# Kernel optimization log

Measured on AMD Instinct MI355X. Metric: run time of the kernel, lower is better.

Reference implementation:

```python
import jax, jax.numpy as jnp
import numpy as np

D = 64
NEG = 0.01            # leakyrelu_neg_slope
X_CONN = 0.25         # x_connection_init
SKIP_H = 0.5          # skip_weight_h
SIGMAS = np.asarray(1.5 ** np.arange(15), np.float32)  # all_sigmas_dist

N_LIG, N_REC = 4096, 8192
E_LIG, E_REC = 65536, 262144
F_LIG, F_REC, NRBF = 15, 27, 15


def _lrelu(x):
    return jax.nn.leaky_relu(x, NEG)


def _ln(x, g, b, eps=1e-5):
    m = x.mean(-1, keepdims=True)
    v = ((x - m) ** 2).mean(-1, keepdims=True)
    return (x - m) * jax.lax.rsqrt(v + eps) * g + b


def _mlp2(x, w1, b1, g, bt, w2, b2):
    # nn.Sequential(Linear, Dropout(0), LeakyReLU, LayerNorm, Linear) in eval mode
    return _ln(_lrelu(x @ w1 + b1), g, bt) @ w2 + b2


def _coords_mlp(m, w1, b1, w2, b2):
    # nn.Sequential(Linear, Dropout(0), LeakyReLU, Linear(out,1))
    return _lrelu(m @ w1 + b1) @ w2 + b2  # [E, 1]


def _seg_mean(v, idx, n):
    # DGL fn.mean over incoming edges at destination nodes (0 for isolated nodes)
    s = jax.ops.segment_sum(v, idx, num_segments=n)
    c = jax.ops.segment_sum(jnp.ones(idx.shape, v.dtype), idx, num_segments=n)
    return s / jnp.maximum(c, 1.0)[:, None]


def setup_inputs() -> dict:
    key = jax.random.key(0)
    ks = iter(jax.random.split(key, 64))

    def n(shape, s=1.0):
        return jax.random.normal(next(ks), shape, jnp.float32) * s

    def lin(i, o):
        return n((i, o), 1.0 / float(np.sqrt(i)))

    zeros = lambda *s: jnp.zeros(s, jnp.float32)
    ones = lambda *s: jnp.ones(s, jnp.float32)

    d = {}
    d['coords_lig'] = n((N_LIG, 3))
    d['h_lig'] = n((N_LIG, D))
    d['orig_h_lig'] = n((N_LIG, D))
    d['orig_coords_lig'] = n((N_LIG, 3))
    d['coords_rec'] = n((N_REC, 3))
    d['h_rec'] = n((N_REC, D))
    d['orig_h_rec'] = n((N_REC, D))
    d['orig_coords_rec'] = n((N_REC, 3))
    d['lig_src'] = jax.random.randint(next(ks), (E_LIG,), 0, N_LIG)
    d['lig_dst'] = jax.random.randint(next(ks), (E_LIG,), 0, N_LIG)
    d['lig_efeat'] = n((E_LIG, F_LIG))
    d['rec_src'] = jax.random.randint(next(ks), (E_REC,), 0, N_REC)
    d['rec_dst'] = jax.random.randint(next(ks), (E_REC,), 0, N_REC)
    d['rec_efeat'] = n((E_REC, F_REC))
    d['mask'] = (jax.random.uniform(next(ks), (N_LIG, N_REC)) < 0.5).astype(jnp.float32)
    # ---- parameters ----
    d['lig_em_w1'], d['lig_em_b1'] = lin(2 * D + F_LIG + NRBF, D), zeros(D)
    d['lig_em_g'], d['lig_em_bt'] = ones(D), zeros(D)
    d['lig_em_w2'], d['lig_em_b2'] = lin(D, D), zeros(D)
    d['rec_em_w1'], d['rec_em_b1'] = lin(2 * D + F_REC + NRBF, D), zeros(D)
    d['rec_em_g'], d['rec_em_bt'] = ones(D), zeros(D)
    d['rec_em_w2'], d['rec_em_b2'] = lin(D, D), zeros(D)
    d['lig_cm_w1'], d['lig_cm_b1'] = lin(D, D), zeros(D)
    d['lig_cm_w2'], d['lig_cm_b2'] = lin(D, 1), zeros(1)
    d['rec_cm_w1'], d['rec_cm_b1'] = lin(D, D), zeros(D)
    d['rec_cm_w2'], d['rec_cm_b2'] = lin(D, 1), zeros(1)
    for nm in ['q_lig_w', 'k_lig_w', 'v_lig_w', 'q_rec_w', 'k_rec_w', 'v_rec_w']:
        d[nm] = lin(D, D)
    d['lig_nm_w1'], d['lig_nm_b1'] = lin(4 * D, D), zeros(D)
    d['lig_nm_g'], d['lig_nm_bt'] = ones(D), zeros(D)
    d['lig_nm_w2'], d['lig_nm_b2'] = lin(D, D), zeros(D)
    d['rec_nm_w1'], d['rec_nm_b1'] = lin(4 * D, D), zeros(D)
    d['rec_nm_g'], d['rec_nm_bt'] = ones(D), zeros(D)
    d['rec_nm_w2'], d['rec_nm_b2'] = lin(D, D), zeros(D)
    return d


def reference(coords_lig, h_lig, orig_h_lig, orig_coords_lig,
              coords_rec, h_rec, orig_h_rec, orig_coords_rec,
              lig_src, lig_dst, lig_efeat, rec_src, rec_dst, rec_efeat, mask,
              lig_em_w1, lig_em_b1, lig_em_g, lig_em_bt, lig_em_w2, lig_em_b2,
              rec_em_w1, rec_em_b1, rec_em_g, rec_em_bt, rec_em_w2, rec_em_b2,
              lig_cm_w1, lig_cm_b1, lig_cm_w2, lig_cm_b2,
              rec_cm_w1, rec_cm_b1, rec_cm_w2, rec_cm_b2,
              q_lig_w, k_lig_w, v_lig_w, q_rec_w, k_rec_w, v_rec_w,
              lig_nm_w1, lig_nm_b1, lig_nm_g, lig_nm_bt, lig_nm_w2, lig_nm_b2,
              rec_nm_w1, rec_nm_b1, rec_nm_g, rec_nm_bt, rec_nm_w2, rec_nm_b2):
    n_lig, n_rec = coords_lig.shape[0], coords_rec.shape[0]
    sig = jnp.asarray(SIGMAS, coords_lig.dtype)

    # --- ligand edge messages: x_rel = x_src - x_dst, multi-scale RBF of |x_rel|^2 ---
    xr_l = coords_lig[lig_src] - coords_lig[lig_dst]                       # [E_l, 3]
    rbf_l = jnp.exp(-jnp.sum(xr_l * xr_l, -1, keepdims=True) / sig)        # [E_l, 15]
    msg_l = _mlp2(jnp.concatenate([h_lig[lig_src], h_lig[lig_dst], lig_efeat, rbf_l], -1),
                  lig_em_w1, lig_em_b1, lig_em_g, lig_em_bt, lig_em_w2, lig_em_b2)

    # --- receptor edge messages (rec_square_distance_scale = 1) ---
    xr_r = coords_rec[rec_src] - coords_rec[rec_dst]
    rbf_r = jnp.exp(-jnp.sum(xr_r * xr_r, -1, keepdims=True) / sig)
    msg_r = _mlp2(jnp.concatenate([h_rec[rec_src], h_rec[rec_dst], rec_efeat, rbf_r], -1),
                  rec_em_w1, rec_em_b1, rec_em_g, rec_em_bt, rec_em_w2, rec_em_b2)

    # --- masked cross-graph attention (pre/post cross-msg norms are identity) ---
    q_l, k_l, v_l = _lrelu(h_lig @ q_lig_w), _lrelu(h_lig @ k_lig_w), h_lig @ v_lig_w
    q_r, k_r, v_r = _lrelu(h_rec @ q_rec_w), _lrelu(h_rec @ k_rec_w), h_rec @ v_rec_w
    s_lr = mask * (q_l @ k_r.T) - 1000.0 * (1.0 - mask)
    att_l = jax.nn.softmax(s_lr, axis=1) @ v_r                             # [N_l, D]
    mt = mask.T
    s_rl = mt * (q_r @ k_l.T) - 1000.0 * (1.0 - mt)
    att_r = jax.nn.softmax(s_rl, axis=1) @ v_l                             # [N_r, D]

    # --- equivariant coordinate update: mean_j phi_x(m_ij) * x_rel, + skip to orig ---
    coef_l = _coords_mlp(msg_l, lig_cm_w1, lig_cm_b1, lig_cm_w2, lig_cm_b2)
    x_lig = X_CONN * orig_coords_lig + (1.0 - X_CONN) * coords_lig + _seg_mean(xr_l * coef_l, lig_dst, n_lig)
    coef_r = _coords_mlp(msg_r, rec_cm_w1, rec_cm_b1, rec_cm_w2, rec_cm_b2)
    x_rec = X_CONN * orig_coords_rec + (1.0 - X_CONN) * coords_rec + _seg_mean(xr_r * coef_r, rec_dst, n_rec)

    # --- node feature update with skip (h_feats_dim == out_feats_dim) ---
    aggr_l = _seg_mean(msg_l, lig_dst, n_lig)
    h_lig_out = SKIP_H * _mlp2(jnp.concatenate([h_lig, aggr_l, att_l, orig_h_lig], -1),
                               lig_nm_w1, lig_nm_b1, lig_nm_g, lig_nm_bt, lig_nm_w2, lig_nm_b2) \
        + (1.0 - SKIP_H) * h_lig
    aggr_r = _seg_mean(msg_r, rec_dst, n_rec)
    h_rec_out = SKIP_H * _mlp2(jnp.concatenate([h_rec, aggr_r, att_r, orig_h_rec], -1),
                               rec_nm_w1, rec_nm_b1, rec_nm_g, rec_nm_bt, rec_nm_w2, rec_nm_b2) \
        + (1.0 - SKIP_H) * h_rec
    return x_lig, h_lig_out, x_rec, h_rec_out
```

## Files before the change

### kernel.cpp

```cpp
#include <hip/hip_runtime.h>
#include <hip/hip_bf16.h>

typedef __hip_bfloat16 bf16;
typedef __attribute__((ext_vector_type(8))) short bfrag8;
typedef __attribute__((ext_vector_type(4))) float f32x4;

#define N_LIG 4096
#define N_REC 8192
#define E_LIG 65536
#define E_REC 262144
#define F_LIGc 15
#define F_RECc 27

__device__ __forceinline__ float ldkv(const float* p, size_t i) { return p[i]; }
__device__ __forceinline__ float ldkv(const bf16* p, size_t i) { return __bfloat162float(p[i]); }
__device__ __forceinline__ short bfbits(float x) {
    bf16 b = __float2bfloat16(x);
    return *(short*)&b;
}
__device__ __forceinline__ unsigned short stg(const float* p, size_t i) {
    return (unsigned short)bfbits(p[i]);
}
__device__ __forceinline__ unsigned short stg(const bf16* p, size_t i) {
    return *(const unsigned short*)(p + i);
}
__device__ __forceinline__ void stage16(unsigned short* d, const bf16* s) {
    *(uint4*)d = *(const uint4*)s;
}
__device__ __forceinline__ void stage16(unsigned short* d, const float* s) {
    float4 a = *(const float4*)s;
    float4 b = *(const float4*)(s + 4);
    unsigned short tmp[8] = {
        (unsigned short)bfbits(a.x), (unsigned short)bfbits(a.y),
        (unsigned short)bfbits(a.z), (unsigned short)bfbits(a.w),
        (unsigned short)bfbits(b.x), (unsigned short)bfbits(b.y),
        (unsigned short)bfbits(b.z), (unsigned short)bfbits(b.w)};
    *(uint4*)d = *(uint4*)tmp;
}

__device__ __forceinline__ int swz(int row, int col) {
    return (row << 6) + ((((col >> 3) ^ row ^ (row >> 3)) & 7) << 3) + (col & 7);
}

__constant__ float c_inv_sigma[15] = {
    1.0f, 0.6666666667f, 0.4444444444f, 0.2962962963f, 0.1975308642f,
    0.1316872428f, 0.08779149520f, 0.05852766346f, 0.03901844231f,
    0.02601229487f, 0.01734152992f, 0.01156101994f, 0.007707346628f,
    0.005138231085f, 0.003425487390f};

__device__ __forceinline__ float wave_sum(float v) {
    #pragma unroll
    for (int o = 32; o > 0; o >>= 1) v += __shfl_xor(v, o, 64);
    return v;
}
__device__ __forceinline__ float quad_max(float v) {
    v = fmaxf(v, __shfl_xor(v, 1)); v = fmaxf(v, __shfl_xor(v, 2));
    v = fmaxf(v, __shfl_xor(v, 4)); v = fmaxf(v, __shfl_xor(v, 8));
    return v;
}
__device__ __forceinline__ float quad_sum(float v) {
    v += __shfl_xor(v, 1); v += __shfl_xor(v, 2);
    v += __shfl_xor(v, 4); v += __shfl_xor(v, 8);
    return v;
}

__global__ void zero_kernel(float* __restrict__ p, int n) {
    int i = blockIdx.x * blockDim.x + threadIdx.x;
    if (i < n) p[i] = 0.f;
}

__global__ void cvt4_kernel(
    const float* __restrict__ a, bf16* __restrict__ oa, int na,
    const float* __restrict__ b, bf16* __restrict__ ob, int nb,
    const float* __restrict__ c, bf16* __restrict__ oc, int nc,
    const float* __restrict__ d, bf16* __restrict__ od, int nd)
{
    int i = blockIdx.x * 256 + threadIdx.x;
    if (i < na) { oa[i] = __float2bfloat16(a[i]); return; }
    i -= na;
    if (i < nb) { ob[i] = __float2bfloat16(b[i]); return; }
    i -= nb;
    if (i < nc) { oc[i] = __float2bfloat16(c[i]); return; }
    i -= nc;
    if (i < nd) od[i] = __float2bfloat16(d[i]);
}

__global__ void hist2_kernel(const int* __restrict__ dl, const int* __restrict__ dr,
                             int* __restrict__ cl, int* __restrict__ cr) {
    int i = blockIdx.x * 256 + threadIdx.x;
    if (i < E_LIG) { atomicAdd(&cl[dl[i]], 1); return; }
    i -= E_LIG;
    if (i < E_REC) atomicAdd(&cr[dr[i]], 1);
}

__global__ __launch_bounds__(256) void scan2_kernel(
    const int* __restrict__ cl, int* __restrict__ curl,
    const int* __restrict__ cr, int* __restrict__ curr)
{
    const int* counts = blockIdx.x ? cr : cl;
    int* cursor = blockIdx.x ? curr : curl;
    int n = blockIdx.x ? N_REC : N_LIG;
    __shared__ int part[256];
    int t = threadIdx.x;
    int c = n / 256;
    int base = t * c;
    int s = 0;
    for (int i = 0; i < c; ++i) s += counts[base + i];
    part[t] = s;
    __syncthreads();
    for (int o = 1; o < 256; o <<= 1) {
        int u = (t >= o) ? part[t - o] : 0;
        __syncthreads();
        part[t] += u;
        __syncthreads();
    }
    int run = part[t] - s;
    for (int i = 0; i < c; ++i) {
        cursor[base + i] = run;
        run += counts[base + i];
    }
}

__global__ void scatter2_kernel(const int* __restrict__ dl, const int* __restrict__ dr,
                                int* __restrict__ curl, int* __restrict__ curr,
                                int* __restrict__ ordl, int* __restrict__ ordr) {
    int i = blockIdx.x * 256 + threadIdx.x;
    if (i < E_LIG) { ordl[atomicAdd(&curl[dl[i]], 1)] = i; return; }
    i -= E_LIG;
    if (i < E_REC) ordr[atomicAdd(&curr[dr[i]], 1)] = i;
}

__global__ __launch_bounds__(256) void pack_frags(
    const float* __restrict__ w_rec1, const float* __restrict__ w_lig1,
    const float* __restrict__ w_rec2, const float* __restrict__ w_lig2,
    const float* __restrict__ c_rec1, const float* __restrict__ c_lig1,
    unsigned short* __restrict__ p_rec1, unsigned short* __restrict__ p_lig1,
    unsigned short* __restrict__ p_rec2, unsigned short* __restrict__ p_lig2,
    unsigned short* __restrict__ pc_rec1, unsigned short* __restrict__ pc_lig1)
{
    int b = blockIdx.x;
    const float* src; unsigned short* dst; int kk, IN;
    if (b < 6)       { src = w_rec1; dst = p_rec1;  kk = b;      IN = 170; }
    else if (b < 11) { src = w_lig1; dst = p_lig1;  kk = b - 6;  IN = 158; }
    else if (b < 13) { src = w_rec2; dst = p_rec2;  kk = b - 11; IN = 64; }
    else if (b < 15) { src = w_lig2; dst = p_lig2;  kk = b - 13; IN = 64; }
    else if (b < 17) { src = c_rec1; dst = pc_rec1; kk = b - 15; IN = 64; }
    else             { src = c_lig1; dst = pc_lig1; kk = b - 17; IN = 64; }
    int t = threadIdx.x, wv = t >> 6, L = t & 63, lm = L & 15, qd = L >> 4;
    int n = wv * 16 + lm;
    unsigned short tmp[8];
    #pragma unroll
    for (int j = 0; j < 8; ++j) {
        int k = kk * 32 + qd * 8 + j;
        tmp[j] = (k < IN) ? (unsigned short)bfbits(src[k * 64 + n]) : (unsigned short)0;
    }
    *(uint4*)&dst[((size_t)(kk * 4 + wv) * 64 + L) * 8] = *(uint4*)tmp;
}

template <int F, int K1S, typename HT>
__global__ __launch_bounds__(256, 5) void edge_mfma(
    const int* __restrict__ order,
    const float* __restrict__ coords, const HT* __restrict__ h,
    const int* __restrict__ src, const int* __restrict__ dst,
    const HT* __restrict__ efeat,
    const unsigned short* __restrict__ w1p, const float* __restrict__ b1,
    const float* __restrict__ g, const float* __restrict__ bt,
    const unsigned short* __restrict__ w2p, const float* __restrict__ b2,
    const unsigned short* __restrict__ c1p, const float* __restrict__ cb1,
    const float* __restrict__ cw2, const float* __restrict__ cb2,
    float* __restrict__ aggr, float* __restrict__ xacc)
{
    constexpr int IN = 143 + F;
    constexpr int KP = K1S * 32 + 8;
    static_assert(64 * KP * 2 >= 64 * 68 * 4, "msgf f32 alias must fit in xb");
    static_assert(64 * KP * 2 >= 64 * 72 * 2, "h1b alias must fit in xb");
    __shared__ __align__(16) char smem[64 * KP * 2];
    __shared__ float wsum1[4][64], wsum2[4][64];
    __shared__ float stat_m[64], stat_r[64];
    __shared__ float coefp[4][64];
    __shared__ float coef_all[64];
    __shared__ int srcs[64], dsts[64], ords[64];
    __shared__ float xr_s[64][3], d2s[64];
    unsigned short* xb   = (unsigned short*)smem;
    unsigned short* h1b  = (unsigned short*)smem;
    float*          msgf = (float*)smem;

    const int t  = threadIdx.x;
    const int wv = t >> 6;
    const int L  = t & 63;
    const int lm = L & 15;
    const int qd = L >> 4;
    const int e0 = blockIdx.x * 64;
    const int n  = wv * 16 + lm;

    bfrag8 w1f[K1S], w2f[2];
    #pragma unroll
    for (int kk = 0; kk < K1S; ++kk)
        w1f[kk] = *(const bfrag8*)&w1p[((size_t)(kk * 4 + wv) * 64 + L) * 8];
    #pragma unroll
    for (int kk = 0; kk < 2; ++kk)
        w2f[kk] = *(const bfrag8*)&w2p[((size_t)(kk * 4 + wv) * 64 + L) * 8];
    const float b1n = b1[n], b2n = b2[n], cb1n = cb1[n], cw2n = cw2[n];
    const float gn = g[n], btn = bt[n];

    if (t < 64) {
        int e = order[e0 + t];
        int s = src[e], d = dst[e];
        ords[t] = e; srcs[t] = s; dsts[t] = d;
        float x0 = coords[s * 3 + 0] - coords[d * 3 + 0];
        float x1 = coords[s * 3 + 1] - coords[d * 3 + 1];
        float x2 = coords[s * 3 + 2] - coords[d * 3 + 2];
        xr_s[t][0] = x0; xr_s[t][1] = x1; xr_s[t][2] = x2;
        d2s[t] = x0 * x0 + x1 * x1 + x2 * x2;
    }
    __syncthreads();

    #pragma unroll
    for (int u = 0; u < 4; ++u) {
        int idx = t + 256 * u;
        int e = idx >> 4, c = idx & 15;
        int node = (c < 8) ? srcs[e] : dsts[e];
        stage16(&xb[e * KP + c * 8], h + (size_t)node * 64 + (c & 7) * 8);
    }
    for (int idx = t; idx < 64 * F; idx += 256) {
        int e = idx / F, f = idx - e * F;
        xb[e * KP + 128 + f] = stg(efeat, (size_t)ords[e] * F + f);
    }
    for (int idx = t; idx < 64 * 15; idx += 256) {
        int e = idx / 15, s5 = idx - e * 15;
        xb[e * KP + 128 + F + s5] = bfbits(__expf(-d2s[e] * c_inv_sigma[s5]));
    }
    {
        constexpr int PER = K1S * 32 - IN;
        for (int idx = t; idx < 64 * PER; idx += 256) {
            int e = idx / PER, k = idx - e * PER;
            xb[e * KP + IN + k] = 0;
        }
    }
    __syncthreads();

    float vreg[4][4];
    #pragma unroll
    for (int m = 0; m < 4; ++m) {
        f32x4 acc = {0.f, 0.f, 0.f, 0.f};
        #pragma unroll
        for (int kk = 0; kk < K1S; ++kk) {
            bfrag8 a = *(const bfrag8*)&xb[(m * 16 + lm) * KP + kk * 32 + qd * 8];
            acc = __builtin_amdgcn_mfma_f32_16x16x32_bf16(a, w1f[kk], acc, 0, 0, 0);
        }
        #pragma unroll
        for (int r = 0; r < 4; ++r) {
            float v = acc[r] + b1n;
            v = v > 0.f ? v : 0.01f * v;
            vreg[m][r] = v;
            float a1 = v, a2 = v * v;
            a1 += __shfl_xor(a1, 1); a2 += __shfl_xor(a2, 1);
            a1 += __shfl_xor(a1, 2); a2 += __shfl_xor(a2, 2);
            a1 += __shfl_xor(a1, 4); a2 += __shfl_xor(a2, 4);
            a1 += __shfl_xor(a1, 8); a2 += __shfl_xor(a2, 8);
            if (lm == 0) {
                wsum1[wv][m * 16 + qd * 4 + r] = a1;
                wsum2[wv][m * 16 + qd * 4 + r] = a2;
            }
        }
    }
    __syncthreads();
    if (t < 64) {
        float s1 = wsum1[0][t] + wsum1[1][t] + wsum1[2][t] + wsum1[3][t];
        float s2 = wsum2[0][t] + wsum2[1][t] + wsum2[2][t] + wsum2[3][t];
        float mean = s1 * (1.f / 64.f);
        float var = s2 * (1.f / 64.f) - mean * mean;
        stat_m[t] = mean;
        stat_r[t] = rsqrtf(fmaxf(var, 0.f) + 1e-5f);
    }
    __syncthreads();

    #pragma unroll
    for (int m = 0; m < 4; ++m)
        #pragma unroll
        for (int r = 0; r < 4; ++r) {
            int row = m * 16 + qd * 4 + r;
            float v = (vreg[m][r] - stat_m[row]) * stat_r[row] * gn + btn;
            h1b[row * 72 + n] = bfbits(v);
        }
    __syncthreads();

    f32x4 acc2[4];
    #pragma unroll
    for (int m = 0; m < 4; ++m) {
        f32x4 acc = {0.f, 0.f, 0.f, 0.f};
        #pragma unroll
        for (int kk = 0; kk < 2; ++kk) {
            bfrag8 a = *(const bfrag8*)&h1b[(m * 16 + lm) * 72 + kk * 32 + qd * 8];
            acc = __builtin_amdgcn_mfma_f32_16x16x32_bf16(a, w2f[kk], acc, 0, 0, 0);
        }
        acc2[m] = acc;
    }
    __syncthreads();
    #pragma unroll
    for (int m = 0; m < 4; ++m)
        #pragma unroll
        for (int r = 0; r < 4; ++r)
            msgf[(m * 16 + qd * 4 + r) * 68 + n] = acc2[m][r] + b2n;
    __syncthreads();

    {
        int j = t & 63, q = t >> 6;
        float acc = 0.f;
        #pragma unroll
        for (int e = q * 16; e < q * 16 + 16; ++e) {
            acc += msgf[e * 68 + j];
            bool flush = (e - q * 16 == 15) || (dsts[e + 1] != dsts[e]);
            if (flush) {
                atomicAdd(&aggr[(size_t)dsts[e] * 64 + j], acc);
                acc = 0.f;
            }
        }
    }

    bfrag8 c1f[2];
    #pragma unroll
    for (int kk = 0; kk < 2; ++kk)
        c1f[kk] = *(const bfrag8*)&c1p[((size_t)(kk * 4 + wv) * 64 + L) * 8];
    #pragma unroll
    for (int m = 0; m < 4; ++m) {
        f32x4 acc = {0.f, 0.f, 0.f, 0.f};
        #pragma unroll
        for (int kk = 0; kk < 2; ++kk) {
            const float* mp = &msgf[(m * 16 + lm) * 68 + kk * 32 + qd * 8];
            f32x4 p0 = *(const f32x4*)mp;
            f32x4 p1 = *(const f32x4*)(mp + 4);
            unsigned short tb[8];
            #pragma unroll
            for (int j = 0; j < 4; ++j) {
                tb[j]     = (unsigned short)bfbits(p0[j]);
                tb[4 + j] = (unsigned short)bfbits(p1[j]);
            }
            bfrag8 a = *(bfrag8*)tb;
            acc = __builtin_amdgcn_mfma_f32_16x16x32_bf16(a, c1f[kk], acc, 0, 0, 0);
        }
        #pragma unroll
        for (int r = 0; r < 4; ++r) {
            float v = acc[r] + cb1n;
            v = v > 0.f ? v : 0.01f * v;
            v *= cw2n;
            v += __shfl_xor(v, 1);
            v += __shfl_xor(v, 2);
            v += __shfl_xor(v, 4);
            v += __shfl_xor(v, 8);
            if (lm == 0) coefp[wv][m * 16 + qd * 4 + r] = v;
        }
    }
    __syncthreads();
    if (t < 64)
        coef_all[t] = coefp[0][t] + coefp[1][t] + coefp[2][t] + coefp[3][t] + cb2[0];
    __syncthreads();

    if (t < 12) {
        int q = t / 3, ax = t - q * 3;
        float acc = 0.f;
        for (int e = q * 16; e < q * 16 + 16; ++e) {
            acc += xr_s[e][ax] * coef_all[e];
            bool flush = (e - q * 16 == 15) || (dsts[e + 1] != dsts[e]);
            if (flush) {
                atomicAdd(&xacc[dsts[e] * 3 + ax], acc);
                acc = 0.f;
            }
        }
    }
}

__global__ __launch_bounds__(256, 3) void node_mfma(
    int nbl,
    const float* h1, const float* __restrict__ aggr1, const int* __restrict__ cnt1,
    const float* att1, const float* __restrict__ origh1,
    const float* __restrict__ w1a, const float* __restrict__ b1a,
    const float* __restrict__ ga, const float* __restrict__ bta,
    const float* __restrict__ w2a, const float* __restrict__ b2a, float* out1,
    const float* h2, const float* __restrict__ aggr2, const int* __restrict__ cnt2,
    const float* att2, const float* __restrict__ origh2,
    const float* __restrict__ w1b, const float* __restrict__ b1b,
    const float* __restrict__ gb, const float* __restrict__ btb,
    const float* __restrict__ w2b, const float* __restrict__ b2b, float* out2)
{
    const float *h, *aggr, *att, *orig_h, *w1, *b1, *g, *bt, *w2, *b2;
    const int* cnt;
    float* h_out;
    int n0;
    if ((int)blockIdx.x < nbl) {
        h = h1; aggr = aggr1; cnt = cnt1; att = att1; orig_h = origh1;
        w1 = w1a; b1 = b1a; g = ga; bt = bta; w2 = w2a; b2 = b2a; h_out = out1;
        n0 = blockIdx.x * 64;
    } else {
        h = h2; aggr = aggr2; cnt = cnt2; att = att2; orig_h = origh2;
        w1 = w1b; b1 = b1b; g = gb; bt = btb; w2 = w2b; b2 = b2b; h_out = out2;
        n0 = (blockIdx.x - nbl) * 64;
    }

    constexpr int KP = 264;
    __shared__ __align__(16) char smem[64 * KP * 2];
    __shared__ __align__(16) unsigned short h1b[64 * 72];
    __shared__ float sums[256], sums2[256];
    __shared__ float stat_m[64], stat_r[64];
    unsigned short* xb  = (unsigned short*)smem;
    float*          h1f = (float*)smem;

    const int t  = threadIdx.x;
    const int lm = t & 15;
    const int qd = (t & 63) >> 4;
    const int n  = (t >> 6) * 16 + lm;

    bfrag8 w1f[8], w2f[2];
    #pragma unroll
    for (int kk = 0; kk < 8; ++kk)
        #pragma unroll
        for (int j = 0; j < 8; ++j) {
            int k = kk * 32 + qd * 8 + j;
            w1f[kk][j] = bfbits(w1[k * 64 + n]);
        }
    #pragma unroll
    for (int kk = 0; kk < 2; ++kk)
        #pragma unroll
        for (int j = 0; j < 8; ++j) {
            int k = kk * 32 + qd * 8 + j;
            w2f[kk][j] = bfbits(w2[k * 64 + n]);
        }
    const float b1n = b1[n], b2n = b2[n];

    for (int p = 0; p < 16; ++p) {
        int e = (t >> 6) + 4 * p;
        int node = n0 + e;
        float invc = 1.f / fmaxf((float)cnt[node], 1.f);
        int j = t & 63;
        xb[e * KP + j]       = bfbits(h[(size_t)node * 64 + j]);
        xb[e * KP + 64 + j]  = bfbits(aggr[(size_t)node * 64 + j] * invc);
        xb[e * KP + 128 + j] = bfbits(att[(size_t)node * 64 + j]);
        xb[e * KP + 192 + j] = bfbits(orig_h[(size_t)node * 64 + j]);
    }
    __syncthreads();

    f32x4 acc1[4];
    #pragma unroll
    for (int m = 0; m < 4; ++m) {
        f32x4 acc = {0.f, 0.f, 0.f, 0.f};
        #pragma unroll
        for (int kk = 0; kk < 8; ++kk) {
            bfrag8 a = *(const bfrag8*)&xb[(m * 16 + lm) * KP + kk * 32 + qd * 8];
            acc = __builtin_amdgcn_mfma_f32_16x16x32_bf16(a, w1f[kk], acc, 0, 0, 0);
        }
        acc1[m] = acc;
    }
    __syncthreads();
    #pragma unroll
    for (int m = 0; m < 4; ++m)
        #pragma unroll
        for (int r = 0; r < 4; ++r) {
            int mr = m * 16 + qd * 4 + r;
            float v = acc1[m][r] + b1n;
            v = v > 0.f ? v : 0.01f * v;
            h1f[mr * 68 + n] = v;
        }
    __syncthreads();

    {
        int e = t >> 2, seg = (t & 3) * 16;
        float s1 = 0.f, s2 = 0.f;
        #pragma unroll
        for (int j = 0; j < 16; ++j) {
            float v = h1f[e * 68 + seg + j];
            s1 += v; s2 += v * v;
        }
        sums[t] = s1; sums2[t] = s2;
    }
    __syncthreads();
    if (t < 64) {
        float s1 = sums[4 * t] + sums[4 * t + 1] + sums[4 * t + 2] + sums[4 * t + 3];
        float s2 = sums2[4 * t] + sums2[4 * t + 1] + sums2[4 * t + 2] + sums2[4 * t + 3];
        float mean = s1 * (1.f / 64.f);
        float var = s2 * (1.f / 64.f) - mean * mean;
        stat_m[t] = mean;
        stat_r[t] = rsqrtf(fmaxf(var, 0.f) + 1e-5f);
    }
    __syncthreads();
    for (int idx = t; idx < 4096; idx += 256) {
        int e = idx >> 6, j = idx & 63;
        float v = (h1f[e * 68 + j] - stat_m[e]) * stat_r[e] * g[j] + bt[j];
        h1b[e * 72 + j] = bfbits(v);
    }
    __syncthreads();

    #pragma unroll
    for (int m = 0; m < 4; ++m) {
        f32x4 acc = {0.f, 0.f, 0.f, 0.f};
        #pragma unroll
        for (int kk = 0; kk < 2; ++kk) {
            bfrag8 a = *(const bfrag8*)&h1b[(m * 16 + lm) * 72 + kk * 32 + qd * 8];
            acc = __builtin_amdgcn_mfma_f32_16x16x32_bf16(a, w2f[kk], acc, 0, 0, 0);
        }
        #pragma unroll
        for (int r = 0; r < 4; ++r) {
            int row = n0 + m * 16 + qd * 4 + r;
            float o = acc[r] + b2n;
            float hv = h[(size_t)row * 64 + n];
            h_out[(size_t)row * 64 + n] = 0.5f * o + 0.5f * hv;
        }
    }
}

__global__ __launch_bounds__(256) void kv_proj_kernel(
    const float* __restrict__ h_lig, const float* __restrict__ h_rec,
    const float* __restrict__ kwl, const float* __restrict__ vwl,
    const float* __restrict__ kwr, const float* __restrict__ vwr,
    bf16* __restrict__ kbl, bf16* __restrict__ vbl,
    bf16* __restrict__ kbr, bf16* __restrict__ vbr)
{
    int job = blockIdx.x * 4 + (threadIdx.x >> 6);
    int j = threadIdx.x & 63;
    const float *h, *w; bf16* out; int node, do_l;
    if (job < N_LIG)                { h = h_lig; w = kwl; out = kbl; node = job;                   do_l = 1; }
    else if (job < 2 * N_LIG)       { h = h_lig; w = vwl; out = vbl; node = job - N_LIG;           do_l = 0; }
    else if (job < 2 * N_LIG + N_REC) { h = h_rec; w = kwr; out = kbr; node = job - 2 * N_LIG;     do_l = 1; }
    else                            { h = h_rec; w = vwr; out = vbr; node = job - 2 * N_LIG - N_REC; do_l = 0; }
    float xv = h[(size_t)node * 64 + j];
    float acc = 0.f;
    #pragma unroll
    for (int i = 0; i < 64; ++i) acc += __shfl(xv, i, 64) * w[i * 64 + j];
    if (do_l) acc = acc > 0.f ? acc : 0.01f * acc;
    out[(size_t)node * 64 + j] = __float2bfloat16(acc);
}

__global__ __launch_bounds__(256) void build_masks(
    const float* __restrict__ mask, unsigned long long* __restrict__ mq,
    unsigned long long* __restrict__ mqT, int R, int C)
{
    __shared__ __align__(4) unsigned char tr[64 * 68];
    __shared__ __align__(4) unsigned char tc[64 * 68];
    int r0 = blockIdx.y * 64, c0 = blockIdx.x * 64;
    int t = threadIdx.x;
    int cs = (t & 15) * 4;
    #pragma unroll
    for (int rr = 0; rr < 4; ++rr) {
        int r = (t >> 4) + rr * 16;
        const float* mp = &mask[(size_t)(r0 + r) * C + c0 + cs];
        unsigned char b0 = mp[0] != 0.f, b1 = mp[1] != 0.f;
        unsigned char b2 = mp[2] != 0.f, b3 = mp[3] != 0.f;
        tr[r * 68 + cs + 0] = b0; tr[r * 68 + cs + 1] = b1;
        tr[r * 68 + cs + 2] = b2; tr[r * 68 + cs + 3] = b3;
        tc[(cs + 0) * 68 + r] = b0; tc[(cs + 1) * 68 + r] = b1;
        tc[(cs + 2) * 68 + r] = b2; tc[(cs + 3) * 68 + r] = b3;
    }
    __syncthreads();
    if (t < 128) {
        const unsigned* p = (t < 64) ? (const unsigned*)&tr[t * 68]
                                     : (const unsigned*)&tc[(t - 64) * 68];
        unsigned lo = 0, hi = 0;
        #pragma unroll
        for (int i = 0; i < 8; ++i)
            lo |= (((p[i] & 0x01010101u) * 0x01020408u) >> 24 & 0xFu) << (4 * i);
        #pragma unroll
        for (int i = 8; i < 16; ++i)
            hi |= (((p[i] & 0x01010101u) * 0x01020408u) >> 24 & 0xFu) << (4 * (i - 8));
        unsigned long long w = (unsigned long long)lo | ((unsigned long long)hi << 32);
        if (t < 64) mq[(size_t)(c0 >> 6) * R + r0 + t] = w;
        else        mqT[(size_t)(r0 >> 6) * C + c0 + (t - 64)] = w;
    }
}

template <int MMODE>
__global__ __launch_bounds__(256, 4) void attn_mfma(
    int nb1,
    const float* __restrict__ h1, const float* __restrict__ qw1,
    const bf16* __restrict__ k1, const bf16* __restrict__ v1,
    const unsigned long long* __restrict__ mq1, const float* __restrict__ mf1, long mrs1, long mcs1,
    float* __restrict__ pO1, float* __restrict__ pM1, float* __restrict__ pL1,
    int nrows1, int ncols1, int nsplit1,
    const float* __restrict__ h2, const float* __restrict__ qw2,
    const bf16* __restrict__ k2, const bf16* __restrict__ v2,
    const unsigned long long* __restrict__ mq2, const float* __restrict__ mf2, long mrs2, long mcs2,
    float* __restrict__ pO2, float* __restrict__ pM2, float* __restrict__ pL2,
    int nrows2, int ncols2, int nsplit2)
{
    const float *h, *qw, *mf;
    const bf16 *kkp, *vvp;
    const unsigned long long* mq;
    long mrs, mcs;
    float *pO, *pM, *pL;
    int n_rows, n_cols, nsplit, bid;
    if ((int)blockIdx.x < nb1) {
        h = h1; qw = qw1; kkp = k1; vvp = v1; mq = mq1; mf = mf1; mrs = mrs1; mcs = mcs1;
        pO = pO1; pM = pM1; pL = pL1; n_rows = nrows1; n_cols = ncols1; nsplit = nsplit1;
        bid = blockIdx.x;
    } else {
        h = h2; qw = qw2; kkp = k2; vvp = v2; mq = mq2; mf = mf2; mrs = mrs2; mcs = mcs2;
        pO = pO2; pM = pM2; pL = pL2; n_rows = nrows2; n_cols = ncols2; nsplit = nsplit2;
        bid = blockIdx.x - nb1;
    }

    const int t  = threadIdx.x;
    const int wv = t >> 6;
    const int lm = t & 15;
    const int qd = (t & 63) >> 4;
    const int rb = bid / nsplit;
    const int sp = bid - rb * nsplit;
    const int r0 = rb * 64;
    const int cols_per = n_cols / nsplit;
    const int c_begin = sp * cols_per;

    __shared__ __align__(16) unsigned short sQ[64 * 64];
    __shared__ __align__(16) unsigned short sP[64 * 64];
    __shared__ __align__(16) unsigned short sK[64 * 64];
    __shared__ __align__(16) unsigned short sV[64 * 64];
    __shared__ uint2 mtq[64];
    __shared__ unsigned char mt[64 * 80];

    const int cP = t >> 3, segP = (t & 7) * 8;

    #pragma unroll
    for (int u = 0; u < 2; ++u) {
        int rr = cP + 32 * u;
        const float* hp = h + (size_t)(r0 + rr) * 64 + segP;
        unsigned short tmp[8];
        #pragma unroll
        for (int j = 0; j < 8; ++j) tmp[j] = bfbits(hp[j]);
        *(uint4*)&sP[swz(rr, segP)] = *(uint4*)tmp;
        const float* qp = qw + (size_t)rr * 64 + segP;
        #pragma unroll
        for (int j = 0; j < 8; ++j) sK[swz(segP + j, rr)] = bfbits(qp[j]);
    }

    uint4 kreg[2], vreg[2];
    unsigned long long mregq = 0;
    kreg[0] = *(const uint4*)(kkp + (size_t)(c_begin + cP) * 64 + segP);
    kreg[1] = *(const uint4*)(kkp + (size_t)(c_begin + cP + 32) * 64 + segP);
    vreg[0] = *(const uint4*)(vvp + (size_t)(c_begin + cP) * 64 + segP);
    vreg[1] = *(const uint4*)(vvp + (size_t)(c_begin + cP + 32) * 64 + segP);
    if (MMODE == 0 && t < 64)
        mregq = mq[(size_t)(c_begin >> 6) * n_rows + r0 + t];
    __syncthreads();

    {
        bfrag8 a0 = *(const bfrag8*)&sP[swz(wv * 16 + lm, qd * 8)];
        bfrag8 a1 = *(const bfrag8*)&sP[swz(wv * 16 + lm, 32 + qd * 8)];
        #pragma unroll
        for (int ns = 0; ns < 4; ++ns) {
            f32x4 acc = {0.f, 0.f, 0.f, 0.f};
            bfrag8 b0 = *(const bfrag8*)&sK[swz(ns * 16 + lm, qd * 8)];
            bfrag8 b1 = *(const bfrag8*)&sK[swz(ns * 16 + lm, 32 + qd * 8)];
            acc = __builtin_amdgcn_mfma_f32_16x16x32_bf16(a0, b0, acc, 0, 0, 0);
            acc = __builtin_amdgcn_mfma_f32_16x16x32_bf16(a1, b1, acc, 0, 0, 0);
            #pragma unroll
            for (int r = 0; r < 4; ++r) {
                float v = acc[r];
                v = v > 0.f ? v : 0.01f * v;
                sQ[swz(wv * 16 + qd * 4 + r, ns * 16 + lm)] = bfbits(v);
            }
        }
    }
    __syncthreads();

    float rm[4], rl[4];
    #pragma unroll
    for (int r = 0; r < 4; ++r) { rm[r] = -1e30f; rl[r] = 0.f; }
    f32x4 o[4];
    #pragma unroll
    for (int ds = 0; ds < 4; ++ds) o[ds] = (f32x4){0.f, 0.f, 0.f, 0.f};

    const int nt = cols_per / 64;
    for (int tile = 0; tile < nt; ++tile) {
        #pragma unroll
        for (int u = 0; u < 2; ++u) {
            int cc = cP + 32 * u;
            *(uint4*)&sK[swz(cc, segP)] = kreg[u];
            unsigned x0 = vreg[u].x, x1 = vreg[u].y, x2 = vreg[u].z, x3 = vreg[u].w;
            sV[swz(segP + 0, cc)] = (unsigned short)x0;
            sV[swz(segP + 1, cc)] = (unsigned short)(x0 >> 16);
            sV[swz(segP + 2, cc)] = (unsigned short)x1;
            sV[swz(segP + 3, cc)] = (unsigned short)(x1 >> 16);
            sV[swz(segP + 4, cc)] = (unsigned short)x2;
            sV[swz(segP + 5, cc)] = (unsigned short)(x2 >> 16);
            sV[swz(segP + 6, cc)] = (unsigned short)x3;
            sV[swz(segP + 7, cc)] = (unsigned short)(x3 >> 16);
        }
        if (MMODE == 0) {
            if (t < 64) mtq[t] = make_uint2((unsigned)mregq, (unsigned)(mregq >> 32));
        } else {
            int c0 = c_begin + tile * 64;
            #pragma unroll
            for (int u = 0; u < 16; ++u) {
                int i = t + 256 * u;
                int r = i >> 6, c = i & 63;
                mt[r * 80 + c] = (unsigned char)(
                    mf[(size_t)(r0 + r) * mrs + (size_t)(c0 + c) * mcs] != 0.f);
            }
        }
        __syncthreads();

        if (tile + 1 < nt) {
            int c0n = c_begin + (tile + 1) * 64;
            kreg[0] = *(const uint4*)(kkp + (size_t)(c0n + cP) * 64 + segP);
            kreg[1] = *(const uint4*)(kkp + (size_t)(c0n + cP + 32) * 64 + segP);
            vreg[0] = *(const uint4*)(vvp + (size_t)(c0n + cP) * 64 + segP);
            vreg[1] = *(const uint4*)(vvp + (size_t)(c0n + cP + 32) * 64 + segP);
            if (MMODE == 0 && t < 64)
                mregq = mq[(size_t)(c0n >> 6) * n_rows + r0 + t];
        }

        f32x4 s[4];
        {
            bfrag8 a0 = *(const bfrag8*)&sQ[swz(wv * 16 + lm, qd * 8)];
            bfrag8 a1 = *(const bfrag8*)&sQ[swz(wv * 16 + lm, 32 + qd * 8)];
            #pragma unroll
            for (int ns = 0; ns < 4; ++ns) {
                f32x4 acc = {0.f, 0.f, 0.f, 0.f};
                bfrag8 b0 = *(const bfrag8*)&sK[swz(ns * 16 + lm, qd * 8)];
                bfrag8 b1 = *(const bfrag8*)&sK[swz(ns * 16 + lm, 32 + qd * 8)];
                acc = __builtin_amdgcn_mfma_f32_16x16x32_bf16(a0, b0, acc, 0, 0, 0);
                acc = __builtin_amdgcn_mfma_f32_16x16x32_bf16(a1, b1, acc, 0, 0, 0);
                s[ns] = acc;
            }
        }

        float alpha[4];
        #pragma unroll
        for (int r = 0; r < 4; ++r) {
            int rloc = wv * 16 + qd * 4 + r;
            float v0, v1, v2, v3;
            if (MMODE == 0) {
                uint2 w = mtq[rloc];
                v0 = (w.x >> lm) & 1        ? s[0][r] : -1000.f;
                v1 = (w.x >> (16 + lm)) & 1 ? s[1][r] : -1000.f;
                v2 = (w.y >> lm) & 1        ? s[2][r] : -1000.f;
                v3 = (w.y >> (16 + lm)) & 1 ? s[3][r] : -1000.f;
            } else {
                v0 = mt[rloc * 80 +  0 + lm] ? s[0][r] : -1000.f;
                v1 = mt[rloc * 80 + 16 + lm] ? s[1][r] : -1000.f;
                v2 = mt[rloc * 80 + 32 + lm] ? s[2][r] : -1000.f;
                v3 = mt[rloc * 80 + 48 + lm] ? s[3][r] : -1000.f;
            }
            float mx = quad_max(fmaxf(fmaxf(v0, v1), fmaxf(v2, v3)));
            float mn = fmaxf(rm[r], mx);
            float al = __expf(rm[r] - mn);
            rm[r] = mn; alpha[r] = al;
            float p0 = __expf(v0 - mn), p1 = __expf(v1 - mn);
            float p2 = __expf(v2 - mn), p3 = __expf(v3 - mn);
            sP[swz(rloc,  0 + lm)] = bfbits(p0);
            sP[swz(rloc, 16 + lm)] = bfbits(p1);
            sP[swz(rloc, 32 + lm)] = bfbits(p2);
            sP[swz(rloc, 48 + lm)] = bfbits(p3);
            float ls = quad_sum(p0 + p1 + p2 + p3);
            rl[r] = rl[r] * al + ls;
        }
        #pragma unroll
        for (int ds = 0; ds < 4; ++ds)
            #pragma unroll
            for (int r = 0; r < 4; ++r) o[ds][r] *= alpha[r];

        __builtin_amdgcn_wave_barrier();
        asm volatile("" ::: "memory");

        {
            bfrag8 a0 = *(const bfrag8*)&sP[swz(wv * 16 + lm, qd * 8)];
            bfrag8 a1 = *(const bfrag8*)&sP[swz(wv * 16 + lm, 32 + qd * 8)];
            #pragma unroll
            for (int ds = 0; ds < 4; ++ds) {
                bfrag8 b0 = *(const bfrag8*)&sV[swz(ds * 16 + lm, qd * 8)];
                bfrag8 b1 = *(const bfrag8*)&sV[swz(ds * 16 + lm, 32 + qd * 8)];
                o[ds] = __builtin_amdgcn_mfma_f32_16x16x32_bf16(a0, b0, o[ds], 0, 0, 0);
                o[ds] = __builtin_amdgcn_mfma_f32_16x16x32_bf16(a1, b1, o[ds], 0, 0, 0);
            }
        }
        __syncthreads();
    }

    #pragma unroll
    for (int ds = 0; ds < 4; ++ds)
        #pragma unroll
        for (int r = 0; r < 4; ++r) {
            int row = r0 + wv * 16 + qd * 4 + r;
            pO[((size_t)sp * n_rows + row) * 64 + ds * 16 + lm] = o[ds][r];
        }
    if (lm == 0) {
        #pragma unroll
        for (int r = 0; r < 4; ++r) {
            int row = r0 + wv * 16 + qd * 4 + r;
            pM[(size_t)sp * n_rows + row] = rm[r];
            pL[(size_t)sp * n_rows + row] = rl[r];
        }
    }
}

__global__ __launch_bounds__(64) void attn_merge2(
    const float* __restrict__ pO1, const float* __restrict__ pM1, const float* __restrict__ pL1,
    float* __restrict__ out1, int ns1,
    const float* __restrict__ pO2, const float* __restrict__ pM2, const float* __restrict__ pL2,
    float* __restrict__ out2, int ns2)
{
    int r = blockIdx.x;
    const float *pO, *pM, *pL; float* out; int n_rows, nsplit;
    if (r < N_LIG) { pO = pO1; pM = pM1; pL = pL1; out = out1; n_rows = N_LIG; nsplit = ns1; }
    else { r -= N_LIG; pO = pO2; pM = pM2; pL = pL2; out = out2; n_rows = N_REC; nsplit = ns2; }
    int d = threadIdx.x;
    float mstar = -1e30f;
    for (int s = 0; s < nsplit; ++s) mstar = fmaxf(mstar, pM[(size_t)s * n_rows + r]);
    float L = 0.f, O = 0.f;
    for (int s = 0; s < nsplit; ++s) {
        float w = __expf(pM[(size_t)s * n_rows + r] - mstar);
        L += pL[(size_t)s * n_rows + r] * w;
        O += pO[((size_t)s * n_rows + r) * 64 + d] * w;
    }
    out[(size_t)r * 64 + d] = O / L;
}

__global__ __launch_bounds__(256) void attn_row_kernel(
    const float* __restrict__ h, const float* __restrict__ qw,
    const bf16* __restrict__ k, const bf16* __restrict__ v,
    const float* __restrict__ mask, long mrs, long mcs,
    float* __restrict__ out, int n_cols)
{
    int row = blockIdx.x;
    int tid = threadIdx.x;
    extern __shared__ float sc[];
    __shared__ float hrow[64];
    __shared__ float qrow[64];
    __shared__ float red[4];
    __shared__ float opart[4][64];

    if (tid < 64) hrow[tid] = h[(size_t)row * 64 + tid];
    __syncthreads();
    if (tid < 64) {
        float a = 0.f;
        #pragma unroll 8
        for (int i = 0; i < 64; ++i) a += hrow[i] * qw[i * 64 + tid];
        qrow[tid] = a > 0.f ? a : 0.01f * a;
    }
    __syncthreads();

    float lmax = -1e30f;
    for (int c = tid; c < n_cols; c += 256) {
        const bf16* kr = k + (size_t)c * 64;
        float s = 0.f;
        #pragma unroll 8
        for (int i = 0; i < 64; ++i) s += qrow[i] * ldkv(kr, i);
        float m = mask[(size_t)row * mrs + (size_t)c * mcs];
        s = m * s - 1000.f * (1.f - m);
        sc[c] = s;
        lmax = fmaxf(lmax, s);
    }
    #pragma unroll
    for (int o = 32; o > 0; o >>= 1) lmax = fmaxf(lmax, __shfl_xor(lmax, o, 64));
    int wid = tid >> 6;
    if ((tid & 63) == 0) red[wid] = lmax;
    __syncthreads();
    float bmax = fmaxf(fmaxf(red[0], red[1]), fmaxf(red[2], red[3]));
    __syncthreads();

    float lsum = 0.f;
    for (int c = tid; c < n_cols; c += 256) {
        float e = __expf(sc[c] - bmax);
        sc[c] = e;
        lsum += e;
    }
    lsum = wave_sum(lsum);
    if ((tid & 63) == 0) red[wid] = lsum;
    __syncthreads();
    float inv = 1.f / (red[0] + red[1] + red[2] + red[3]);

    int dd = tid & 63;
    float o = 0.f;
    for (int c = wid; c < n_cols; c += 4) o += sc[c] * ldkv(v, (size_t)c * 64 + dd);
    opart[wid][dd] = o;
    __syncthreads();
    if (wid == 0)
        out[(size_t)row * 64 + dd] =
            (opart[0][dd] + opart[1][dd] + opart[2][dd] + opart[3][dd]) * inv;
}

__global__ void coord2_kernel(
    const float* __restrict__ ol, const float* __restrict__ cl,
    const float* __restrict__ xl, const int* __restrict__ cntl, float* __restrict__ outl,
    const float* __restrict__ orr, const float* __restrict__ cr,
    const float* __restrict__ xr, const int* __restrict__ cntr, float* __restrict__ outr)
{
    int i = blockIdx.x * 256 + threadIdx.x;
    if (i < N_LIG * 3) {
        int node = i / 3;
        float invc = 1.f / fmaxf((float)cntl[node], 1.f);
        outl[i] = 0.25f * ol[i] + 0.75f * cl[i] + xl[i] * invc;
        return;
    }
    i -= N_LIG * 3;
    if (i < N_REC * 3) {
        int node = i / 3;
        float invc = 1.f / fmaxf((float)cntr[node], 1.f);
        outr[i] = 0.25f * orr[i] + 0.75f * cr[i] + xr[i] * invc;
    }
}

extern "C" void kernel_launch(void* const* d_in, const int* in_sizes, int n_in,
                              void* d_out, int out_size, void* d_ws, size_t ws_size,
                              hipStream_t stream)
{
    const float* coords_lig      = (const float*)d_in[0];
    const float* h_lig           = (const float*)d_in[1];
    const float* orig_h_lig      = (const float*)d_in[2];
    const float* orig_coords_lig = (const float*)d_in[3];
    const float* coords_rec      = (const float*)d_in[4];
    const float* h_rec           = (const float*)d_in[5];
    const float* orig_h_rec      = (const float*)d_in[6];
    const float* orig_coords_rec = (const float*)d_in[7];
    const int* lig_src   = (const int*)d_in[8];
    const int* lig_dst   = (const int*)d_in[9];
    const float* lig_efeat = (const float*)d_in[10];
    const int* rec_src   = (const int*)d_in[11];
    const int* rec_dst   = (const int*)d_in[12];
    const float* rec_efeat = (const float*)d_in[13];
    const float* mask      = (const float*)d_in[14];
    const float *lig_em_w1 = (const float*)d_in[15], *lig_em_b1 = (const float*)d_in[16];
    const float *lig_em_g  = (const float*)d_in[17], *lig_em_bt = (const float*)d_in[18];
    const float *lig_em_w2 = (const float*)d_in[19], *lig_em_b2 = (const float*)d_in[20];
    const float *rec_em_w1 = (const float*)d_in[21], *rec_em_b1 = (const float*)d_in[22];
    const float *rec_em_g  = (const float*)d_in[23], *rec_em_bt = (const float*)d_in[24];
    const float *rec_em_w2 = (const float*)d_in[25], *rec_em_b2 = (const float*)d_in[26];
    const float *lig_cm_w1 = (const float*)d_in[27], *lig_cm_b1 = (const float*)d_in[28];
    const float *lig_cm_w2 = (const float*)d_in[29], *lig_cm_b2 = (const float*)d_in[30];
    const float *rec_cm_w1 = (const float*)d_in[31], *rec_cm_b1 = (const float*)d_in[32];
    const float *rec_cm_w2 = (const float*)d_in[33], *rec_cm_b2 = (const float*)d_in[34];
    const float *q_lig_w = (const float*)d_in[35], *k_lig_w = (const float*)d_in[36];
    const float *v_lig_w = (const float*)d_in[37], *q_rec_w = (const float*)d_in[38];
    const float *k_rec_w = (const float*)d_in[39], *v_rec_w = (const float*)d_in[40];
    const float *lig_nm_w1 = (const float*)d_in[41], *lig_nm_b1 = (const float*)d_in[42];
    const float *lig_nm_g  = (const float*)d_in[43], *lig_nm_bt = (const float*)d_in[44];
    const float *lig_nm_w2 = (const float*)d_in[45], *lig_nm_b2 = (const float*)d_in[46];
    const float *rec_nm_w1 = (const float*)d_in[47], *rec_nm_b1 = (const float*)d_in[48];
    const float *rec_nm_g  = (const float*)d_in[49], *rec_nm_bt = (const float*)d_in[50];
    const float *rec_nm_w2 = (const float*)d_in[51], *rec_nm_b2 = (const float*)d_in[52];

    char* wsb = (char*)d_ws;
    float* aggr_l = (float*)(wsb + 16);
    float* aggr_r = aggr_l + (size_t)N_LIG * 64;
    float* xacc_l = aggr_r + (size_t)N_REC * 64;
    float* xacc_r = xacc_l + (size_t)N_LIG * 3;
    int* counts_l = (int*)(xacc_r + (size_t)N_REC * 3);
    int* counts_r = counts_l + N_LIG;
    const size_t zero_floats =
        (size_t)N_LIG * 64 + (size_t)N_REC * 64 + N_LIG * 3 + N_REC * 3 + N_LIG + N_REC;
    int* cursor_l = counts_r + N_REC;
    int* cursor_r = cursor_l + N_LIG;
    int* order_l  = cursor_r + N_REC;
    int* order_r  = order_l + E_LIG;
    unsigned short* p_rec1  = (unsigned short*)(order_r + E_REC);
    unsigned short* p_lig1  = p_rec1 + 6 * 2048;
    unsigned short* p_rec2  = p_lig1 + 5 * 2048;
    unsigned short* p_lig2  = p_rec2 + 2 * 2048;
    unsigned short* pc_rec1 = p_lig2 + 2 * 2048;
    unsigned short* pc_lig1 = pc_rec1 + 2 * 2048;
    char* kv_base = (char*)(pc_lig1 + 2 * 2048);
    const size_t core_b = (size_t)(kv_base - wsb);
    const size_t kv_b = (size_t)(N_LIG + N_REC) * 64 * 2 * 2;

    const size_t mq1_n = (size_t)(N_REC / 64) * N_LIG;
    const size_t mq2_n = (size_t)(N_LIG / 64) * N_REC;
    const size_t mq_all_b = (mq1_n + mq2_n) * 8;
    const size_t mir_b = (size_t)(N_LIG + N_REC) * 64 * 2
                       + ((size_t)E_LIG * F_LIGc + (size_t)E_REC * F_RECc) * 2;
    const size_t region_b = mir_b > mq_all_b ? mir_b : mq_all_b;

    const size_t part_b_hi = ((size_t)8 * N_LIG * 64 + (size_t)4 * N_REC * 64) * 4
                           + ((size_t)8 * N_LIG + (size_t)4 * N_REC) * 2 * 4;
    const size_t part_b_lo = ((size_t)4 * N_LIG * 64 + (size_t)2 * N_REC * 64) * 4
                           + ((size_t)4 * N_LIG + (size_t)2 * N_REC) * 2 * 4;

    int tier, ns1, ns2;
    size_t part_b;
    if (ws_size >= core_b + kv_b + part_b_hi + region_b) {
        tier = 0; ns1 = 8; ns2 = 4; part_b = part_b_hi;
    } else if (ws_size >= core_b + kv_b + part_b_lo + region_b) {
        tier = 0; ns1 = 4; ns2 = 2; part_b = part_b_lo;
    } else if (ws_size >= core_b + kv_b + part_b_lo) {
        tier = 1; ns1 = 4; ns2 = 2; part_b = part_b_lo;
    } else {
        tier = 2; ns1 = 4; ns2 = 2; part_b = part_b_lo;
    }

    bf16* kb_l = (bf16*)kv_base;
    bf16* vb_l = kb_l + (size_t)N_LIG * 64;
    bf16* kb_r = vb_l + (size_t)N_LIG * 64;
    bf16* vb_r = kb_r + (size_t)N_REC * 64;
    float* pO1 = (float*)(kv_base + kv_b);
    float* pO2 = pO1 + (size_t)ns1 * N_LIG * 64;
    float* pM1 = pO2 + (size_t)ns2 * N_REC * 64;
    float* pL1 = pM1 + (size_t)ns1 * N_LIG;
    float* pM2 = pL1 + (size_t)ns1 * N_LIG;
    float* pL2 = pM2 + (size_t)ns2 * N_REC;
    unsigned long long* mqb  = (unsigned long long*)(kv_base + kv_b + part_b);
    unsigned long long* mqbT = mqb + mq1_n;
    bf16* hb_l  = (bf16*)mqb;
    bf16* hb_r  = hb_l + (size_t)N_LIG * 64;
    bf16* efb_l = hb_r + (size_t)N_REC * 64;
    bf16* efb_r = efb_l + (size_t)E_LIG * F_LIGc;

    float* out = (float*)d_out;
    float* x_lig_o = out;
    float* h_lig_o = out + 12288;
    float* x_rec_o = out + 274432;
    float* h_rec_o = out + 299008;

    zero_kernel<<<((int)zero_floats + 255) / 256, 256, 0, stream>>>(aggr_l, (int)zero_floats);

    pack_frags<<<19, 256, 0, stream>>>(
        rec_em_w1, lig_em_w1, rec_em_w2, lig_em_w2, rec_cm_w1, lig_cm_w1,
        p_rec1, p_lig1, p_rec2, p_lig2, pc_rec1, pc_lig1);

    hist2_kernel<<<(E_LIG + E_REC) / 256, 256, 0, stream>>>(lig_dst, rec_dst, counts_l, counts_r);
    scan2_kernel<<<2, 256, 0, stream>>>(counts_l, cursor_l, counts_r, cursor_r);
    scatter2_kernel<<<(E_LIG + E_REC) / 256, 256, 0, stream>>>(
        lig_dst, rec_dst, cursor_l, cursor_r, order_l, order_r);

    kv_proj_kernel<<<(2 * (N_LIG + N_REC)) / 4, 256, 0, stream>>>(
        h_lig, h_rec, k_lig_w, v_lig_w, k_rec_w, v_rec_w,
        kb_l, vb_l, kb_r, vb_r);

    if (tier == 0) {
        cvt4_kernel<<<(N_LIG * 64 + N_REC * 64 + E_LIG * F_LIGc + E_REC * F_RECc + 255) / 256,
                      256, 0, stream>>>(
            h_lig, hb_l, N_LIG * 64, h_rec, hb_r, N_REC * 64,
            lig_efeat, efb_l, E_LIG * F_LIGc, rec_efeat, efb_r, E_REC * F_RECc);
        edge_mfma<F_LIGc, 5, bf16><<<E_LIG / 64, 256, 0, stream>>>(
            order_l, coords_lig, hb_l, lig_src, lig_dst, efb_l,
            p_lig1, lig_em_b1, lig_em_g, lig_em_bt, p_lig2, lig_em_b2,
            pc_lig1, lig_cm_b1, lig_cm_w2, lig_cm_b2,
            aggr_l, xacc_l);
        edge_mfma<F_RECc, 6, bf16><<<E_REC / 64, 256, 0, stream>>>(
            order_r, coords_rec, hb_r, rec_src, rec_dst, efb_r,
            p_rec1, rec_em_b1, rec_em_g, rec_em_bt, p_rec2, rec_em_b2,
            pc_rec1, rec_cm_b1, rec_cm_w2, rec_cm_b2,
            aggr_r, xacc_r);
    } else {
        edge_mfma<F_LIGc, 5, float><<<E_LIG / 64, 256, 0, stream>>>(
            order_l, coords_lig, h_lig, lig_src, lig_dst, lig_efeat,
            p_lig1, lig_em_b1, lig_em_g, lig_em_bt, p_lig2, lig_em_b2,
            pc_lig1, lig_cm_b1, lig_cm_w2, lig_cm_b2,
            aggr_l, xacc_l);
        edge_mfma<F_RECc, 6, float><<<E_REC / 64, 256, 0, stream>>>(
            order_r, coords_rec, h_rec, rec_src, rec_dst, rec_efeat,
            p_rec1, rec_em_b1, rec_em_g, rec_em_bt, p_rec2, rec_em_b2,
            pc_rec1, rec_cm_b1, rec_cm_w2, rec_cm_b2,
            aggr_r, xacc_r);
    }

    const int nb1 = (N_LIG / 64) * ns1;
    const int nb2 = (N_REC / 64) * ns2;
    if (tier <= 1) {
        if (tier == 0) {
            dim3 bg(N_REC / 64, N_LIG / 64);
            build_masks<<<bg, 256, 0, stream>>>(mask, mqb, mqbT, N_LIG, N_REC);
            attn_mfma<0><<<nb1 + nb2, 256, 0, stream>>>(
                nb1,
                h_lig, q_lig_w, kb_r, vb_r, mqb, mask, 0L, 0L,
                pO1, pM1, pL1, N_LIG, N_REC, ns1,
                h_rec, q_rec_w, kb_l, vb_l, mqbT, mask, 0L, 0L,
                pO2, pM2, pL2, N_REC, N_LIG, ns2);
        } else {
            attn_mfma<1><<<nb1 + nb2, 256, 0, stream>>>(
                nb1,
                h_lig, q_lig_w, kb_r, vb_r, (const unsigned long long*)0, mask, (long)N_REC, 1L,
                pO1, pM1, pL1, N_LIG, N_REC, ns1,
                h_rec, q_rec_w, kb_l, vb_l, (const unsigned long long*)0, mask, 1L, (long)N_REC,
                pO2, pM2, pL2, N_REC, N_LIG, ns2);
        }
        attn_merge2<<<N_LIG + N_REC, 64, 0, stream>>>(
            pO1, pM1, pL1, h_lig_o, ns1, pO2, pM2, pL2, h_rec_o, ns2);
    } else {
        attn_row_kernel<<<N_LIG, 256, N_REC * sizeof(float), stream>>>(
            h_lig, q_lig_w, kb_r, vb_r, mask, (long)N_REC, 1L, h_lig_o, N_REC);
        attn_row_kernel<<<N_REC, 256, N_LIG * sizeof(float), stream>>>(
            h_rec, q_rec_w, kb_l, vb_l, mask, 1L, (long)N_REC, h_rec_o, N_LIG);
    }

    node_mfma<<<N_LIG / 64 + N_REC / 64, 256, 0, stream>>>(
        N_LIG / 64,
        h_lig, aggr_l, counts_l, h_lig_o, orig_h_lig,
        lig_nm_w1, lig_nm_b1, lig_nm_g, lig_nm_bt, lig_nm_w2, lig_nm_b2, h_lig_o,
        h_rec, aggr_r, counts_r, h_rec_o, orig_h_rec,
        rec_nm_w1, rec_nm_b1, rec_nm_g, rec_nm_bt, rec_nm_w2, rec_nm_b2, h_rec_o);

    coord2_kernel<<<((N_LIG + N_REC) * 3 + 255) / 256, 256, 0, stream>>>(
        orig_coords_lig, coords_lig, xacc_l, counts_l, x_lig_o,
        orig_coords_rec, coords_rec, xacc_r, counts_r, x_rec_o);
}
```

Measured before the change: 608.4 us.

## Fuse edge and attention work into one persistent mega kernel with shared smem

Turns the edge MLP and masked attention kernels into device functions that share one dynamic shared buffer, and launches them from a single mega_kernel so the edge and attention blocks run concurrently on the GPU. The attention row-sum is now computed with an extra MFMA against a ones vector instead of shuffle reductions. The split count for attention doubles, build_masks moves earlier, and the coordinate update is folded into node_mfma. The aim is to remove launch gaps and tail underutilisation. The cost is higher register and LDS pressure from the merged kernel, plus extra partial buffers to merge.

```diff
diff --git a/kernel.cpp b/kernel.cpp
--- a/kernel.cpp
+++ b/kernel.cpp
@@ -56,11 +56,6 @@
 __device__ __forceinline__ float quad_max(float v) {
     v = fmaxf(v, __shfl_xor(v, 1)); v = fmaxf(v, __shfl_xor(v, 2));
     v = fmaxf(v, __shfl_xor(v, 4)); v = fmaxf(v, __shfl_xor(v, 8));
-    return v;
-}
-__device__ __forceinline__ float quad_sum(float v) {
-    v += __shfl_xor(v, 1); v += __shfl_xor(v, 2);
-    v += __shfl_xor(v, 4); v += __shfl_xor(v, 8);
     return v;
 }
 
@@ -158,7 +153,8 @@
 }
 
 template <int F, int K1S, typename HT>
-__global__ __launch_bounds__(256, 5) void edge_mfma(
+__device__ __forceinline__ void edge_body(
+    char* sbuf, int ebid,
     const int* __restrict__ order,
     const float* __restrict__ coords, const HT* __restrict__ h,
     const int* __restrict__ src, const int* __restrict__ dst,
@@ -172,25 +168,30 @@
 {
     constexpr int IN = 143 + F;
     constexpr int KP = K1S * 32 + 8;
-    static_assert(64 * KP * 2 >= 64 * 68 * 4, "msgf f32 alias must fit in xb");
-    static_assert(64 * KP * 2 >= 64 * 72 * 2, "h1b alias must fit in xb");
-    __shared__ __align__(16) char smem[64 * KP * 2];
-    __shared__ float wsum1[4][64], wsum2[4][64];
-    __shared__ float stat_m[64], stat_r[64];
-    __shared__ float coefp[4][64];
-    __shared__ float coef_all[64];
-    __shared__ int srcs[64], dsts[64], ords[64];
-    __shared__ float xr_s[64][3], d2s[64];
-    unsigned short* xb   = (unsigned short*)smem;
-    unsigned short* h1b  = (unsigned short*)smem;
-    float*          msgf = (float*)smem;
+    constexpr int XB = 64 * KP * 2;
+    static_assert(XB >= 64 * 68 * 4, "msgf f32 alias must fit in xb");
+    static_assert(XB >= 64 * 72 * 2, "h1b alias must fit in xb");
+    unsigned short* xb   = (unsigned short*)sbuf;
+    unsigned short* h1b  = (unsigned short*)sbuf;
+    float*          msgf = (float*)sbuf;
+    float* wsum1   = (float*)(sbuf + XB);
+    float* wsum2   = (float*)(sbuf + XB + 1024);
+    float* stat_m  = (float*)(sbuf + XB + 2048);
+    float* stat_r  = (float*)(sbuf + XB + 2304);
+    float* coefp   = (float*)(sbuf + XB + 2560);
+    float* coef_all= (float*)(sbuf + XB + 3584);
+    int*   srcs    = (int*)(sbuf + XB + 3840);
+    int*   dsts    = (int*)(sbuf + XB + 4096);
+    int*   ords    = (int*)(sbuf + XB + 4352);
+    float* xr_s    = (float*)(sbuf + XB + 4608);
+    float* d2s     = (float*)(sbuf + XB + 5376);
 
     const int t  = threadIdx.x;
     const int wv = t >> 6;
     const int L  = t & 63;
     const int lm = L & 15;
     const int qd = L >> 4;
-    const int e0 = blockIdx.x * 64;
+    const int e0 = ebid * 64;
     const int n  = wv * 16 + lm;
 
     bfrag8 w1f[K1S], w2f[2];
@@ -210,7 +211,7 @@
         float x0 = coords[s * 3 + 0] - coords[d * 3 + 0];
         float x1 = coords[s * 3 + 1] - coords[d * 3 + 1];
         float x2 = coords[s * 3 + 2] - coords[d * 3 + 2];
-        xr_s[t][0] = x0; xr_s[t][1] = x1; xr_s[t][2] = x2;
+        xr_s[t * 3 + 0] = x0; xr_s[t * 3 + 1] = x1; xr_s[t * 3 + 2] = x2;
         d2s[t] = x0 * x0 + x1 * x1 + x2 * x2;
     }
     __syncthreads();
@@ -259,15 +260,15 @@
             a1 += __shfl_xor(a1, 4); a2 += __shfl_xor(a2, 4);
             a1 += __shfl_xor(a1, 8); a2 += __shfl_xor(a2, 8);
             if (lm == 0) {
-                wsum1[wv][m * 16 + qd * 4 + r] = a1;
-                wsum2[wv][m * 16 + qd * 4 + r] = a2;
+                wsum1[wv * 64 + m * 16 + qd * 4 + r] = a1;
+                wsum2[wv * 64 + m * 16 + qd * 4 + r] = a2;
             }
         }
     }
     __syncthreads();
     if (t < 64) {
-        float s1 = wsum1[0][t] + wsum1[1][t] + wsum1[2][t] + wsum1[3][t];
-        float s2 = wsum2[0][t] + wsum2[1][t] + wsum2[2][t] + wsum2[3][t];
+        float s1 = wsum1[t] + wsum1[64 + t] + wsum1[128 + t] + wsum1[192 + t];
+        float s2 = wsum2[t] + wsum2[64 + t] + wsum2[128 + t] + wsum2[192 + t];
         float mean = s1 * (1.f / 64.f);
         float var = s2 * (1.f / 64.f) - mean * mean;
         stat_m[t] = mean;
@@ -348,19 +349,19 @@
             v += __shfl_xor(v, 2);
             v += __shfl_xor(v, 4);
             v += __shfl_xor(v, 8);
-            if (lm == 0) coefp[wv][m * 16 + qd * 4 + r] = v;
+            if (lm == 0) coefp[wv * 64 + m * 16 + qd * 4 + r] = v;
         }
     }
     __syncthreads();
     if (t < 64)
-        coef_all[t] = coefp[0][t] + coefp[1][t] + coefp[2][t] + coefp[3][t] + cb2[0];
+        coef_all[t] = coefp[t] + coefp[64 + t] + coefp[128 + t] + coefp[192 + t] + cb2[0];
     __syncthreads();
 
     if (t < 12) {
         int q = t / 3, ax = t - q * 3;
         float acc = 0.f;
         for (int e = q * 16; e < q * 16 + 16; ++e) {
-            acc += xr_s[e][ax] * coef_all[e];
+            acc += xr_s[e * 3 + ax] * coef_all[e];
             bool flush = (e - q * 16 == 15) || (dsts[e + 1] != dsts[e]);
             if (flush) {
                 atomicAdd(&xacc[dsts[e] * 3 + ax], acc);
@@ -370,205 +371,9 @@
     }
 }
 
-__global__ __launch_bounds__(256, 3) void node_mfma(
-    int nbl,
-    const float* h1, const float* __restrict__ aggr1, const int* __restrict__ cnt1,
-    const float* att1, const float* __restrict__ origh1,
-    const float* __restrict__ w1a, const float* __restrict__ b1a,
-    const float* __restrict__ ga, const float* __restrict__ bta,
-    const float* __restrict__ w2a, const float* __restrict__ b2a, float* out1,
-    const float* h2, const float* __restrict__ aggr2, const int* __restrict__ cnt2,
-    const float* att2, const float* __restrict__ origh2,
-    const float* __restrict__ w1b, const float* __restrict__ b1b,
-    const float* __restrict__ gb, const float* __restrict__ btb,
-    const float* __restrict__ w2b, const float* __restrict__ b2b, float* out2)
-{
-    const float *h, *aggr, *att, *orig_h, *w1, *b1, *g, *bt, *w2, *b2;
-    const int* cnt;
-    float* h_out;
-    int n0;
-    if ((int)blockIdx.x < nbl) {
-        h = h1; aggr = aggr1; cnt = cnt1; att = att1; orig_h = origh1;
-        w1 = w1a; b1 = b1a; g = ga; bt = bta; w2 = w2a; b2 = b2a; h_out = out1;
-        n0 = blockIdx.x * 64;
-    } else {
-        h = h2; aggr = aggr2; cnt = cnt2; att = att2; orig_h = origh2;
-        w1 = w1b; b1 = b1b; g = gb; bt = btb; w2 = w2b; b2 = b2b; h_out = out2;
-        n0 = (blockIdx.x - nbl) * 64;
-    }
-
-    constexpr int KP = 264;
-    __shared__ __align__(16) char smem[64 * KP * 2];
-    __shared__ __align__(16) unsigned short h1b[64 * 72];
-    __shared__ float sums[256], sums2[256];
-    __shared__ float stat_m[64], stat_r[64];
-    unsigned short* xb  = (unsigned short*)smem;
-    float*          h1f = (float*)smem;
-
-    const int t  = threadIdx.x;
-    const int lm = t & 15;
-    const int qd = (t & 63) >> 4;
-    const int n  = (t >> 6) * 16 + lm;
-
-    bfrag8 w1f[8], w2f[2];
-    #pragma unroll
-    for (int kk = 0; kk < 8; ++kk)
-        #pragma unroll
-        for (int j = 0; j < 8; ++j) {
-            int k = kk * 32 + qd * 8 + j;
-            w1f[kk][j] = bfbits(w1[k * 64 + n]);
-        }
-    #pragma unroll
-    for (int kk = 0; kk < 2; ++kk)
-        #pragma unroll
-        for (int j = 0; j < 8; ++j) {
-            int k = kk * 32 + qd * 8 + j;
-            w2f[kk][j] = bfbits(w2[k * 64 + n]);
-        }
-    const float b1n = b1[n], b2n = b2[n];
-
-    for (int p = 0; p < 16; ++p) {
-        int e = (t >> 6) + 4 * p;
-        int node = n0 + e;
-        float invc = 1.f / fmaxf((float)cnt[node], 1.f);
-        int j = t & 63;
-        xb[e * KP + j]       = bfbits(h[(size_t)node * 64 + j]);
-        xb[e * KP + 64 + j]  = bfbits(aggr[(size_t)node * 64 + j] * invc);
-        xb[e * KP + 128 + j] = bfbits(att[(size_t)node * 64 + j]);
-        xb[e * KP + 192 + j] = bfbits(orig_h[(size_t)node * 64 + j]);
-    }
-    __syncthreads();
-
-    f32x4 acc1[4];
-    #pragma unroll
-    for (int m = 0; m < 4; ++m) {
-        f32x4 acc = {0.f, 0.f, 0.f, 0.f};
-        #pragma unroll
-        for (int kk = 0; kk < 8; ++kk) {
-            bfrag8 a = *(const bfrag8*)&xb[(m * 16 + lm) * KP + kk * 32 + qd * 8];
-            acc = __builtin_amdgcn_mfma_f32_16x16x32_bf16(a, w1f[kk], acc, 0, 0, 0);
-        }
-        acc1[m] = acc;
-    }
-    __syncthreads();
-    #pragma unroll
-    for (int m = 0; m < 4; ++m)
-        #pragma unroll
-        for (int r = 0; r < 4; ++r) {
-            int mr = m * 16 + qd * 4 + r;
-            float v = acc1[m][r] + b1n;
-            v = v > 0.f ? v : 0.01f * v;
-            h1f[mr * 68 + n] = v;
-        }
-    __syncthreads();
-
-    {
-        int e = t >> 2, seg = (t & 3) * 16;
-        float s1 = 0.f, s2 = 0.f;
-        #pragma unroll
-        for (int j = 0; j < 16; ++j) {
-            float v = h1f[e * 68 + seg + j];
-            s1 += v; s2 += v * v;
-        }
-        sums[t] = s1; sums2[t] = s2;
-    }
-    __syncthreads();
-    if (t < 64) {
-        float s1 = sums[4 * t] + sums[4 * t + 1] + sums[4 * t + 2] + sums[4 * t + 3];
-        float s2 = sums2[4 * t] + sums2[4 * t + 1] + sums2[4 * t + 2] + sums2[4 * t + 3];
-        float mean = s1 * (1.f / 64.f);
-        float var = s2 * (1.f / 64.f) - mean * mean;
-        stat_m[t] = mean;
-        stat_r[t] = rsqrtf(fmaxf(var, 0.f) + 1e-5f);
-    }
-    __syncthreads();
-    for (int idx = t; idx < 4096; idx += 256) {
-        int e = idx >> 6, j = idx & 63;
-        float v = (h1f[e * 68 + j] - stat_m[e]) * stat_r[e] * g[j] + bt[j];
-        h1b[e * 72 + j] = bfbits(v);
-    }
-    __syncthreads();
-
-    #pragma unroll
-    for (int m = 0; m < 4; ++m) {
-        f32x4 acc = {0.f, 0.f, 0.f, 0.f};
-        #pragma unroll
-        for (int kk = 0; kk < 2; ++kk) {
-            bfrag8 a = *(const bfrag8*)&h1b[(m * 16 + lm) * 72 + kk * 32 + qd * 8];
-            acc = __builtin_amdgcn_mfma_f32_16x16x32_bf16(a, w2f[kk], acc, 0, 0, 0);
-        }
-        #pragma unroll
-        for (int r = 0; r < 4; ++r) {
-            int row = n0 + m * 16 + qd * 4 + r;
-            float o = acc[r] + b2n;
-            float hv = h[(size_t)row * 64 + n];
-            h_out[(size_t)row * 64 + n] = 0.5f * o + 0.5f * hv;
-        }
-    }
-}
-
-__global__ __launch_bounds__(256) void kv_proj_kernel(
-    const float* __restrict__ h_lig, const float* __restrict__ h_rec,
-    const float* __restrict__ kwl, const float* __restrict__ vwl,
-    const float* __restrict__ kwr, const float* __restrict__ vwr,
-    bf16* __restrict__ kbl, bf16* __restrict__ vbl,
-    bf16* __restrict__ kbr, bf16* __restrict__ vbr)
-{
-    int job = blockIdx.x * 4 + (threadIdx.x >> 6);
-    int j = threadIdx.x & 63;
-    const float *h, *w; bf16* out; int node, do_l;
-    if (job < N_LIG)                { h = h_lig; w = kwl; out = kbl; node = job;                   do_l = 1; }
-    else if (job < 2 * N_LIG)       { h = h_lig; w = vwl; out = vbl; node = job - N_LIG;           do_l = 0; }
-    else if (job < 2 * N_LIG + N_REC) { h = h_rec; w = kwr; out = kbr; node = job - 2 * N_LIG;     do_l = 1; }
-    else                            { h = h_rec; w = vwr; out = vbr; node = job - 2 * N_LIG - N_REC; do_l = 0; }
-    float xv = h[(size_t)node * 64 + j];
-    float acc = 0.f;
-    #pragma unroll
-    for (int i = 0; i < 64; ++i) acc += __shfl(xv, i, 64) * w[i * 64 + j];
-    if (do_l) acc = acc > 0.f ? acc : 0.01f * acc;
-    out[(size_t)node * 64 + j] = __float2bfloat16(acc);
-}
-
-__global__ __launch_bounds__(256) void build_masks(
-    const float* __restrict__ mask, unsigned long long* __restrict__ mq,
-    unsigned long long* __restrict__ mqT, int R, int C)
-{
-    __shared__ __align__(4) unsigned char tr[64 * 68];
-    __shared__ __align__(4) unsigned char tc[64 * 68];
-    int r0 = blockIdx.y * 64, c0 = blockIdx.x * 64;
-    int t = threadIdx.x;
-    int cs = (t & 15) * 4;
-    #pragma unroll
-    for (int rr = 0; rr < 4; ++rr) {
-        int r = (t >> 4) + rr * 16;
-        const float* mp = &mask[(size_t)(r0 + r) * C + c0 + cs];
-        unsigned char b0 = mp[0] != 0.f, b1 = mp[1] != 0.f;
-        unsigned char b2 = mp[2] != 0.f, b3 = mp[3] != 0.f;
-        tr[r * 68 + cs + 0] = b0; tr[r * 68 + cs + 1] = b1;
-        tr[r * 68 + cs + 2] = b2; tr[r * 68 + cs + 3] = b3;
-        tc[(cs + 0) * 68 + r] = b0; tc[(cs + 1) * 68 + r] = b1;
-        tc[(cs + 2) * 68 + r] = b2; tc[(cs + 3) * 68 + r] = b3;
-    }
-    __syncthreads();
-    if (t < 128) {
-        const unsigned* p = (t < 64) ? (const unsigned*)&tr[t * 68]
-                                     : (const unsigned*)&tc[(t - 64) * 68];
-        unsigned lo = 0, hi = 0;
-        #pragma unroll
-        for (int i = 0; i < 8; ++i)
-            lo |= (((p[i] & 0x01010101u) * 0x01020408u) >> 24 & 0xFu) << (4 * i);
-        #pragma unroll
-        for (int i = 8; i < 16; ++i)
-            hi |= (((p[i] & 0x01010101u) * 0x01020408u) >> 24 & 0xFu) << (4 * (i - 8));
-        unsigned long long w = (unsigned long long)lo | ((unsigned long long)hi << 32);
-        if (t < 64) mq[(size_t)(c0 >> 6) * R + r0 + t] = w;
-        else        mqT[(size_t)(r0 >> 6) * C + c0 + (t - 64)] = w;
-    }
-}
-
 template <int MMODE>
-__global__ __launch_bounds__(256, 4) void attn_mfma(
-    int nb1,
+__device__ __forceinline__ void attn_body(
+    char* sbuf, int bid, int nb1,
     const float* __restrict__ h1, const float* __restrict__ qw1,
     const bf16* __restrict__ k1, const bf16* __restrict__ v1,
     const unsigned long long* __restrict__ mq1, const float* __restrict__ mf1, long mrs1, long mcs1,
@@ -585,16 +390,22 @@
     const unsigned long long* mq;
     long mrs, mcs;
     float *pO, *pM, *pL;
-    int n_rows, n_cols, nsplit, bid;
-    if ((int)blockIdx.x < nb1) {
+    int n_rows, n_cols, nsplit;
+    if (bid < nb1) {
         h = h1; qw = qw1; kkp = k1; vvp = v1; mq = mq1; mf = mf1; mrs = mrs1; mcs = mcs1;
         pO = pO1; pM = pM1; pL = pL1; n_rows = nrows1; n_cols = ncols1; nsplit = nsplit1;
-        bid = blockIdx.x;
     } else {
         h = h2; qw = qw2; kkp = k2; vvp = v2; mq = mq2; mf = mf2; mrs = mrs2; mcs = mcs2;
         pO = pO2; pM = pM2; pL = pL2; n_rows = nrows2; n_cols = ncols2; nsplit = nsplit2;
-        bid = blockIdx.x - nb1;
-    }
+        bid -= nb1;
+    }
+
+    unsigned short* sQ = (unsigned short*)sbuf;
+    unsigned short* sP = (unsigned short*)(sbuf + 8192);
+    unsigned short* sK = (unsigned short*)(sbuf + 16384);
+    unsigned short* sV = (unsigned short*)(sbuf + 24576);
+    uint2* mtq = (uint2*)(sbuf + 32768);
+    unsigned char* mt = (unsigned char*)(sbuf + 32768);
 
     const int t  = threadIdx.x;
     const int wv = t >> 6;
@@ -605,13 +416,6 @@
     const int r0 = rb * 64;
     const int cols_per = n_cols / nsplit;
     const int c_begin = sp * cols_per;
-
-    __shared__ __align__(16) unsigned short sQ[64 * 64];
-    __shared__ __align__(16) unsigned short sP[64 * 64];
-    __shared__ __align__(16) unsigned short sK[64 * 64];
-    __shared__ __align__(16) unsigned short sV[64 * 64];
-    __shared__ uint2 mtq[64];
-    __shared__ unsigned char mt[64 * 80];
 
     const int cP = t >> 3, segP = (t & 7) * 8;
 
@@ -658,12 +462,15 @@
     }
     __syncthreads();
 
-    float rm[4], rl[4];
-    #pragma unroll
-    for (int r = 0; r < 4; ++r) { rm[r] = -1e30f; rl[r] = 0.f; }
+    float rm[4];
+    #pragma unroll
+    for (int r = 0; r < 4; ++r) rm[r] = -1e30f;
     f32x4 o[4];
     #pragma unroll
     for (int ds = 0; ds < 4; ++ds) o[ds] = (f32x4){0.f, 0.f, 0.f, 0.f};
+    f32x4 osum = {0.f, 0.f, 0.f, 0.f};
+    const short ONE = (short)0x3F80;
+    const bfrag8 bones = {ONE, ONE, ONE, ONE, ONE, ONE, ONE, ONE};
 
     const int nt = cols_per / 64;
     for (int tile = 0; tile < nt; ++tile) {
@@ -747,8 +554,7 @@
             sP[swz(rloc, 16 + lm)] = bfbits(p1);
             sP[swz(rloc, 32 + lm)] = bfbits(p2);
             sP[swz(rloc, 48 + lm)] = bfbits(p3);
-            float ls = quad_sum(p0 + p1 + p2 + p3);
-            rl[r] = rl[r] * al + ls;
+            osum[r] *= al;
         }
         #pragma unroll
         for (int ds = 0; ds < 4; ++ds)
@@ -768,6 +574,8 @@
                 o[ds] = __builtin_amdgcn_mfma_f32_16x16x32_bf16(a0, b0, o[ds], 0, 0, 0);
                 o[ds] = __builtin_amdgcn_mfma_f32_16x16x32_bf16(a1, b1, o[ds], 0, 0, 0);
             }
+            osum = __builtin_amdgcn_mfma_f32_16x16x32_bf16(a0, bones, osum, 0, 0, 0);
+            osum = __builtin_amdgcn_mfma_f32_16x16x32_bf16(a1, bones, osum, 0, 0, 0);
         }
         __syncthreads();
     }
@@ -784,8 +592,295 @@
         for (int r = 0; r < 4; ++r) {
             int row = r0 + wv * 16 + qd * 4 + r;
             pM[(size_t)sp * n_rows + row] = rm[r];
-            pL[(size_t)sp * n_rows + row] = rl[r];
-        }
+            pL[(size_t)sp * n_rows + row] = osum[r];
+        }
+    }
+}
+
+__global__ __launch_bounds__(256, 4) void mega_kernel(
+    int nb1,
+    const float* h1, const float* qw1, const bf16* k1, const bf16* v1,
+    const unsigned long long* mq1, float* pO1, float* pM1, float* pL1,
+    int nrows1, int ncols1, int ns1,
+    const float* h2, const float* qw2, const bf16* k2, const bf16* v2,
+    const unsigned long long* mq2, float* pO2, float* pM2, float* pL2,
+    int nrows2, int ncols2, int ns2,
+    const int* ordR, const float* coordsR, const bf16* hR,
+    const int* srcR, const int* dstR, const bf16* efR,
+    const unsigned short* w1pR, const float* b1R, const float* gR, const float* btR,
+    const unsigned short* w2pR, const float* b2R,
+    const unsigned short* c1pR, const float* cb1R, const float* cw2R, const float* cb2R,
+    float* aggrR, float* xaccR,
+    const int* ordL, const float* coordsL, const bf16* hL,
+    const int* srcL, const int* dstL, const bf16* efL,
+    const unsigned short* w1pL, const float* b1L, const float* gL, const float* btL,
+    const unsigned short* w2pL, const float* b2L,
+    const unsigned short* c1pL, const float* cb1L, const float* cw2L, const float* cb2L,
+    float* aggrL, float* xaccL)
+{
+    __shared__ __align__(16) char sbuf[33280];
+    int bid = blockIdx.x;
+    int g7 = bid / 7, r7 = bid - g7 * 7;
+    if (r7 < 2) {
+        attn_body<0>(sbuf, g7 * 2 + r7, nb1,
+            h1, qw1, k1, v1, mq1, (const float*)0, 0L, 0L, pO1, pM1, pL1, nrows1, ncols1, ns1,
+            h2, qw2, k2, v2, mq2, (const float*)0, 0L, 0L, pO2, pM2, pL2, nrows2, ncols2, ns2);
+    } else {
+        int eid = g7 * 5 + (r7 - 2);
+        if (eid < E_REC / 64)
+            edge_body<F_RECc, 6, bf16>(sbuf, eid, ordR, coordsR, hR, srcR, dstR, efR,
+                w1pR, b1R, gR, btR, w2pR, b2R, c1pR, cb1R, cw2R, cb2R, aggrR, xaccR);
+        else
+            edge_body<F_LIGc, 5, bf16>(sbuf, eid - E_REC / 64, ordL, coordsL, hL, srcL, dstL, efL,
+                w1pL, b1L, gL, btL, w2pL, b2L, c1pL, cb1L, cw2L, cb2L, aggrL, xaccL);
+    }
+}
+
+template <int F, int K1S>
+__global__ __launch_bounds__(256, 4) void edge_mfma_f(
+    const int* order, const float* coords, const float* h,
+    const int* src, const int* dst, const float* efeat,
+    const unsigned short* w1p, const float* b1, const float* g, const float* bt,
+    const unsigned short* w2p, const float* b2,
+    const unsigned short* c1p, const float* cb1, const float* cw2, const float* cb2,
+    float* aggr, float* xacc)
+{
+    __shared__ __align__(16) char sbuf[64 * (K1S * 32 + 8) * 2 + 5632];
+    edge_body<F, K1S, float>(sbuf, blockIdx.x, order, coords, h, src, dst, efeat,
+        w1p, b1, g, bt, w2p, b2, c1p, cb1, cw2, cb2, aggr, xacc);
+}
+
+__global__ __launch_bounds__(256, 4) void attn_f32mask(
+    int nb1,
+    const float* h1, const float* qw1, const bf16* k1, const bf16* v1,
+    const float* mf1, long mrs1, long mcs1,
+    float* pO1, float* pM1, float* pL1, int nrows1, int ncols1, int ns1,
+    const float* h2, const float* qw2, const bf16* k2, const bf16* v2,
+    const float* mf2, long mrs2, long mcs2,
+    float* pO2, float* pM2, float* pL2, int nrows2, int ncols2, int ns2)
+{
+    __shared__ __align__(16) char sbuf[37888];
+    attn_body<1>(sbuf, blockIdx.x, nb1,
+        h1, qw1, k1, v1, (const unsigned long long*)0, mf1, mrs1, mcs1,
+        pO1, pM1, pL1, nrows1, ncols1, ns1,
+        h2, qw2, k2, v2, (const unsigned long long*)0, mf2, mrs2, mcs2,
+        pO2, pM2, pL2, nrows2, ncols2, ns2);
+}
+
+__global__ __launch_bounds__(256, 3) void node_mfma(
+    int nbl, int nbn,
+    const float* h1, const float* __restrict__ aggr1, const int* __restrict__ cnt1,
+    const float* att1, const float* __restrict__ origh1,
+    const float* __restrict__ w1a, const float* __restrict__ b1a,
+    const float* __restrict__ ga, const float* __restrict__ bta,
+    const float* __restrict__ w2a, const float* __restrict__ b2a, float* out1,
+    const float* h2, const float* __restrict__ aggr2, const int* __restrict__ cnt2,
+    const float* att2, const float* __restrict__ origh2,
+    const float* __restrict__ w1b, const float* __restrict__ b1b,
+    const float* __restrict__ gb, const float* __restrict__ btb,
+    const float* __restrict__ w2b, const float* __restrict__ b2b, float* out2,
+    const float* __restrict__ ocl, const float* __restrict__ ccl,
+    const float* __restrict__ xaccl, float* __restrict__ outxl,
+    const float* __restrict__ ocr, const float* __restrict__ ccr,
+    const float* __restrict__ xaccr, float* __restrict__ outxr)
+{
+    if ((int)blockIdx.x >= nbn) {
+        int i = (blockIdx.x - nbn) * 256 + threadIdx.x;
+        if (i < N_LIG * 3) {
+            int node = i / 3;
+            float invc = 1.f / fmaxf((float)cnt1[node], 1.f);
+            outxl[i] = 0.25f * ocl[i] + 0.75f * ccl[i] + xaccl[i] * invc;
+        } else {
+            i -= N_LIG * 3;
+            if (i < N_REC * 3) {
+                int node = i / 3;
+                float invc = 1.f / fmaxf((float)cnt2[node], 1.f);
+                outxr[i] = 0.25f * ocr[i] + 0.75f * ccr[i] + xaccr[i] * invc;
+            }
+        }
+        return;
+    }
+
+    const float *h, *aggr, *att, *orig_h, *w1, *b1, *g, *bt, *w2, *b2;
+    const int* cnt;
+    float* h_out;
+    int n0;
+    if ((int)blockIdx.x < nbl) {
+        h = h1; aggr = aggr1; cnt = cnt1; att = att1; orig_h = origh1;
+        w1 = w1a; b1 = b1a; g = ga; bt = bta; w2 = w2a; b2 = b2a; h_out = out1;
+        n0 = blockIdx.x * 64;
+    } else {
+        h = h2; aggr = aggr2; cnt = cnt2; att = att2; orig_h = origh2;
+        w1 = w1b; b1 = b1b; g = gb; bt = btb; w2 = w2b; b2 = b2b; h_out = out2;
+        n0 = (blockIdx.x - nbl) * 64;
+    }
+
+    constexpr int KP = 264;
+    __shared__ __align__(16) char smem[64 * KP * 2];
+    __shared__ __align__(16) unsigned short h1b[64 * 72];
+    __shared__ float sums[256], sums2[256];
+    __shared__ float stat_m[64], stat_r[64];
+    unsigned short* xb  = (unsigned short*)smem;
+    float*          h1f = (float*)smem;
+
+    const int t  = threadIdx.x;
+    const int lm = t & 15;
+    const int qd = (t & 63) >> 4;
+    const int n  = (t >> 6) * 16 + lm;
+
+    bfrag8 w1f[8], w2f[2];
+    #pragma unroll
+    for (int kk = 0; kk < 8; ++kk)
+        #pragma unroll
+        for (int j = 0; j < 8; ++j) {
+            int k = kk * 32 + qd * 8 + j;
+            w1f[kk][j] = bfbits(w1[k * 64 + n]);
+        }
+    #pragma unroll
+    for (int kk = 0; kk < 2; ++kk)
+        #pragma unroll
+        for (int j = 0; j < 8; ++j) {
+            int k = kk * 32 + qd * 8 + j;
+            w2f[kk][j] = bfbits(w2[k * 64 + n]);
+        }
+    const float b1n = b1[n], b2n = b2[n];
+
+    for (int p = 0; p < 16; ++p) {
+        int e = (t >> 6) + 4 * p;
+        int node = n0 + e;
+        float invc = 1.f / fmaxf((float)cnt[node], 1.f);
+        int j = t & 63;
+        xb[e * KP + j]       = bfbits(h[(size_t)node * 64 + j]);
+        xb[e * KP + 64 + j]  = bfbits(aggr[(size_t)node * 64 + j] * invc);
+        xb[e * KP + 128 + j] = bfbits(att[(size_t)node * 64 + j]);
+        xb[e * KP + 192 + j] = bfbits(orig_h[(size_t)node * 64 + j]);
+    }
+    __syncthreads();
+
+    f32x4 acc1[4];
+    #pragma unroll
+    for (int m = 0; m < 4; ++m) {
+        f32x4 acc = {0.f, 0.f, 0.f, 0.f};
+        #pragma unroll
+        for (int kk = 0; kk < 8; ++kk) {
+            bfrag8 a = *(const bfrag8*)&xb[(m * 16 + lm) * KP + kk * 32 + qd * 8];
+            acc = __builtin_amdgcn_mfma_f32_16x16x32_bf16(a, w1f[kk], acc, 0, 0, 0);
+        }
+        acc1[m] = acc;
+    }
+    __syncthreads();
+    #pragma unroll
+    for (int m = 0; m < 4; ++m)
+        #pragma unroll
+        for (int r = 0; r < 4; ++r) {
+            int mr = m * 16 + qd * 4 + r;
+            float v = acc1[m][r] + b1n;
+            v = v > 0.f ? v : 0.01f * v;
+            h1f[mr * 68 + n] = v;
+        }
+    __syncthreads();
+
+    {
+        int e = t >> 2, seg = (t & 3) * 16;
+        float s1 = 0.f, s2 = 0.f;
+        #pragma unroll
+        for (int j = 0; j < 16; ++j) {
+            float v = h1f[e * 68 + seg + j];
+            s1 += v; s2 += v * v;
+        }
+        sums[t] = s1; sums2[t] = s2;
+    }
+    __syncthreads();
+    if (t < 64) {
+        float s1 = sums[4 * t] + sums[4 * t + 1] + sums[4 * t + 2] + sums[4 * t + 3];
+        float s2 = sums2[4 * t] + sums2[4 * t + 1] + sums2[4 * t + 2] + sums2[4 * t + 3];
+        float mean = s1 * (1.f / 64.f);
+        float var = s2 * (1.f / 64.f) - mean * mean;
+        stat_m[t] = mean;
+        stat_r[t] = rsqrtf(fmaxf(var, 0.f) + 1e-5f);
+    }
+    __syncthreads();
+    for (int idx = t; idx < 4096; idx += 256) {
+        int e = idx >> 6, j = idx & 63;
+        float v = (h1f[e * 68 + j] - stat_m[e]) * stat_r[e] * g[j] + bt[j];
+        h1b[e * 72 + j] = bfbits(v);
+    }
+    __syncthreads();
+
+    #pragma unroll
+    for (int m = 0; m < 4; ++m) {
+        f32x4 acc = {0.f, 0.f, 0.f, 0.f};
+        #pragma unroll
+        for (int kk = 0; kk < 2; ++kk) {
+            bfrag8 a = *(const bfrag8*)&h1b[(m * 16 + lm) * 72 + kk * 32 + qd * 8];
+            acc = __builtin_amdgcn_mfma_f32_16x16x32_bf16(a, w2f[kk], acc, 0, 0, 0);
+        }
+        #pragma unroll
+        for (int r = 0; r < 4; ++r) {
+            int row = n0 + m * 16 + qd * 4 + r;
+            float o = acc[r] + b2n;
+            float hv = h[(size_t)row * 64 + n];
+            h_out[(size_t)row * 64 + n] = 0.5f * o + 0.5f * hv;
+        }
+    }
+}
+
+__global__ __launch_bounds__(256) void kv_proj_kernel(
+    const float* __restrict__ h_lig, const float* __restrict__ h_rec,
+    const float* __restrict__ kwl, const float* __restrict__ vwl,
+    const float* __restrict__ kwr, const float* __restrict__ vwr,
+    bf16* __restrict__ kbl, bf16* __restrict__ vbl,
+    bf16* __restrict__ kbr, bf16* __restrict__ vbr)
+{
+    int job = blockIdx.x * 4 + (threadIdx.x >> 6);
+    int j = threadIdx.x & 63;
+    const float *h, *w; bf16* out; int node, do_l;
+    if (job < N_LIG)                { h = h_lig; w = kwl; out = kbl; node = job;                   do_l = 1; }
+    else if (job < 2 * N_LIG)       { h = h_lig; w = vwl; out = vbl; node = job - N_LIG;           do_l = 0; }
+    else if (job < 2 * N_LIG + N_REC) { h = h_rec; w = kwr; out = kbr; node = job - 2 * N_LIG;     do_l = 1; }
+    else                            { h = h_rec; w = vwr; out = vbr; node = job - 2 * N_LIG - N_REC; do_l = 0; }
+    float xv = h[(size_t)node * 64 + j];
+    float acc = 0.f;
+    #pragma unroll
+    for (int i = 0; i < 64; ++i) acc += __shfl(xv, i, 64) * w[i * 64 + j];
+    if (do_l) acc = acc > 0.f ? acc : 0.01f * acc;
+    out[(size_t)node * 64 + j] = __float2bfloat16(acc);
+}
+
+__global__ __launch_bounds__(256) void build_masks(
+    const float* __restrict__ mask, unsigned long long* __restrict__ mq,
+    unsigned long long* __restrict__ mqT, int R, int C)
+{
+    __shared__ __align__(4) unsigned char tr[64 * 68];
+    __shared__ __align__(4) unsigned char tc[64 * 68];
+    int r0 = blockIdx.y * 64, c0 = blockIdx.x * 64;
+    int t = threadIdx.x;
+    int cs = (t & 15) * 4;
+    #pragma unroll
+    for (int rr = 0; rr < 4; ++rr) {
+        int r = (t >> 4) + rr * 16;
+        const float* mp = &mask[(size_t)(r0 + r) * C + c0 + cs];
+        unsigned char b0 = mp[0] != 0.f, b1 = mp[1] != 0.f;
+        unsigned char b2 = mp[2] != 0.f, b3 = mp[3] != 0.f;
+        tr[r * 68 + cs + 0] = b0; tr[r * 68 + cs + 1] = b1;
+        tr[r * 68 + cs + 2] = b2; tr[r * 68 + cs + 3] = b3;
+        tc[(cs + 0) * 68 + r] = b0; tc[(cs + 1) * 68 + r] = b1;
+        tc[(cs + 2) * 68 + r] = b2; tc[(cs + 3) * 68 + r] = b3;
+    }
+    __syncthreads();
+    if (t < 128) {
+        const unsigned* p = (t < 64) ? (const unsigned*)&tr[t * 68]
+                                     : (const unsigned*)&tc[(t - 64) * 68];
+        unsigned lo = 0, hi = 0;
+        #pragma unroll
+        for (int i = 0; i < 8; ++i)
+            lo |= (((p[i] & 0x01010101u) * 0x01020408u) >> 24 & 0xFu) << (4 * i);
+        #pragma unroll
+        for (int i = 8; i < 16; ++i)
+            hi |= (((p[i] & 0x01010101u) * 0x01020408u) >> 24 & 0xFu) << (4 * (i - 8));
+        unsigned long long w = (unsigned long long)lo | ((unsigned long long)hi << 32);
+        if (t < 64) mq[(size_t)(c0 >> 6) * R + r0 + t] = w;
+        else        mqT[(size_t)(r0 >> 6) * C + c0 + (t - 64)] = w;
     }
 }
 
@@ -873,27 +968,6 @@
     if (wid == 0)
         out[(size_t)row * 64 + dd] =
             (opart[0][dd] + opart[1][dd] + opart[2][dd] + opart[3][dd]) * inv;
-}
-
-__global__ void coord2_kernel(
-    const float* __restrict__ ol, const float* __restrict__ cl,
-    const float* __restrict__ xl, const int* __restrict__ cntl, float* __restrict__ outl,
-    const float* __restrict__ orr, const float* __restrict__ cr,
-    const float* __restrict__ xr, const int* __restrict__ cntr, float* __restrict__ outr)
-{
-    int i = blockIdx.x * 256 + threadIdx.x;
-    if (i < N_LIG * 3) {
-        int node = i / 3;
-        float invc = 1.f / fmaxf((float)cntl[node], 1.f);
-        outl[i] = 0.25f * ol[i] + 0.75f * cl[i] + xl[i] * invc;
-        return;
-    }
-    i -= N_LIG * 3;
-    if (i < N_REC * 3) {
-        int node = i / 3;
-        float invc = 1.f / fmaxf((float)cntr[node], 1.f);
-        outr[i] = 0.25f * orr[i] + 0.75f * cr[i] + xr[i] * invc;
-    }
 }
 
 extern "C" void kernel_launch(void* const* d_in, const int* in_sizes, int n_in,
@@ -963,19 +1037,16 @@
     const size_t mq_all_b = (mq1_n + mq2_n) * 8;
     const size_t mir_b = (size_t)(N_LIG + N_REC) * 64 * 2
                        + ((size_t)E_LIG * F_LIGc + (size_t)E_REC * F_RECc) * 2;
-    const size_t region_b = mir_b > mq_all_b ? mir_b : mq_all_b;
-
-    const size_t part_b_hi = ((size_t)8 * N_LIG * 64 + (size_t)4 * N_REC * 64) * 4
-                           + ((size_t)8 * N_LIG + (size_t)4 * N_REC) * 2 * 4;
+
+    const size_t part_b_hi = ((size_t)16 * N_LIG * 64 + (size_t)8 * N_REC * 64) * 4
+                           + ((size_t)16 * N_LIG + (size_t)8 * N_REC) * 2 * 4;
     const size_t part_b_lo = ((size_t)4 * N_LIG * 64 + (size_t)2 * N_REC * 64) * 4
                            + ((size_t)4 * N_LIG + (size_t)2 * N_REC) * 2 * 4;
 
     int tier, ns1, ns2;
     size_t part_b;
-    if (ws_size >= core_b + kv_b + part_b_hi + region_b) {
-        tier = 0; ns1 = 8; ns2 = 4; part_b = part_b_hi;
-    } else if (ws_size >= core_b + kv_b + part_b_lo + region_b) {
-        tier = 0; ns1 = 4; ns2 = 2; part_b = part_b_lo;
+    if (ws_size >= core_b + kv_b + part_b_hi + mq_all_b + mir_b) {
+        tier = 0; ns1 = 16; ns2 = 8; part_b = part_b_hi;
     } else if (ws_size >= core_b + kv_b + part_b_lo) {
         tier = 1; ns1 = 4; ns2 = 2; part_b = part_b_lo;
     } else {
@@ -994,7 +1065,7 @@
     float* pL2 = pM2 + (size_t)ns2 * N_REC;
     unsigned long long* mqb  = (unsigned long long*)(kv_base + kv_b + part_b);
     unsigned long long* mqbT = mqb + mq1_n;
-    bf16* hb_l  = (bf16*)mqb;
+    bf16* hb_l  = (bf16*)(mqbT + mq2_n);
     bf16* hb_r  = hb_l + (size_t)N_LIG * 64;
     bf16* efb_l = hb_r + (size_t)N_REC * 64;
     bf16* efb_r = efb_l + (size_t)E_LIG * F_LIGc;
@@ -1007,6 +1078,11 @@
 
     zero_kernel<<<((int)zero_floats + 255) / 256, 256, 0, stream>>>(aggr_l, (int)zero_floats);
 
+    if (tier == 0) {
+        dim3 bg(N_REC / 64, N_LIG / 64);
+        build_masks<<<bg, 256, 0, stream>>>(mask, mqb, mqbT, N_LIG, N_REC);
+    }
+
     pack_frags<<<19, 256, 0, stream>>>(
         rec_em_w1, lig_em_w1, rec_em_w2, lig_em_w2, rec_cm_w1, lig_cm_w1,
         p_rec1, p_lig1, p_rec2, p_lig2, pc_rec1, pc_lig1);
@@ -1019,72 +1095,63 @@
     kv_proj_kernel<<<(2 * (N_LIG + N_REC)) / 4, 256, 0, stream>>>(
         h_lig, h_rec, k_lig_w, v_lig_w, k_rec_w, v_rec_w,
         kb_l, vb_l, kb_r, vb_r);
+
+    const int nb1 = (N_LIG / 64) * ns1;
+    const int nb2 = (N_REC / 64) * ns2;
 
     if (tier == 0) {
         cvt4_kernel<<<(N_LIG * 64 + N_REC * 64 + E_LIG * F_LIGc + E_REC * F_RECc + 255) / 256,
                       256, 0, stream>>>(
             h_lig, hb_l, N_LIG * 64, h_rec, hb_r, N_REC * 64,
             lig_efeat, efb_l, E_LIG * F_LIGc, rec_efeat, efb_r, E_REC * F_RECc);
-        edge_mfma<F_LIGc, 5, bf16><<<E_LIG / 64, 256, 0, stream>>>(
+
+        mega_kernel<<<7 * 1024, 256, 0, stream>>>(
+            nb1,
+            h_lig, q_lig_w, kb_r, vb_r, mqb, pO1, pM1, pL1, N_LIG, N_REC, ns1,
+            h_rec, q_rec_w, kb_l, vb_l, mqbT, pO2, pM2, pL2, N_REC, N_LIG, ns2,
+            order_r, coords_rec, hb_r, rec_src, rec_dst, efb_r,
+            p_rec1, rec_em_b1, rec_em_g, rec_em_bt, p_rec2, rec_em_b2,
+            pc_rec1, rec_cm_b1, rec_cm_w2, rec_cm_b2, aggr_r, xacc_r,
             order_l, coords_lig, hb_l, lig_src, lig_dst, efb_l,
             p_lig1, lig_em_b1, lig_em_g, lig_em_bt, p_lig2, lig_em_b2,
-            pc_lig1, lig_cm_b1, lig_cm_w2, lig_cm_b2,
-            aggr_l, xacc_l);
-        edge_mfma<F_RECc, 6, bf16><<<E_REC / 64, 256, 0, stream>>>(
-            order_r, coords_rec, hb_r, rec_src, rec_dst, efb_r,
-            p_rec1, rec_em_b1, rec_em_g, rec_em_bt, p_rec2, rec_em_b2,
-            pc_rec1, rec_cm_b1, rec_cm_w2, rec_cm_b2,
-            aggr_r, xacc_r);
-    } else {
-        edge_mfma<F_LIGc, 5, float><<<E_LIG / 64, 256, 0, stream>>>(
-            order_l, coords_lig, h_lig, lig_src, lig_dst, lig_efeat,
-            p_lig1, lig_em_b1, lig_em_g, lig_em_bt, p_lig2, lig_em_b2,
-            pc_lig1, lig_cm_b1, lig_cm_w2, lig_cm_b2,
-            aggr_l, xacc_l);
-        edge_mfma<F_RECc, 6, float><<<E_REC / 64, 256, 0, stream>>>(
-            order_r, coords_rec, h_rec, rec_src, rec_dst, rec_efeat,
-            p_rec1, rec_em_b1, rec_em_g, rec_em_bt, p_rec2, rec_em_b2,
-            pc_rec1, rec_cm_b1, rec_cm_w2, rec_cm_b2,
-            aggr_r, xacc_r);
-    }
-
-    const int nb1 = (N_LIG / 64) * ns1;
-    const int nb2 = (N_REC / 64) * ns2;
-    if (tier <= 1) {
-        if (tier == 0) {
-            dim3 bg(N_REC / 64, N_LIG / 64);
-            build_masks<<<bg, 256, 0, stream>>>(mask, mqb, mqbT, N_LIG, N_REC);
-            attn_mfma<0><<<nb1 + nb2, 256, 0, stream>>>(
-                nb1,
-                h_lig, q_lig_w, kb_r, vb_r, mqb, mask, 0L, 0L,
-                pO1, pM1, pL1, N_LIG, N_REC, ns1,
-                h_rec, q_rec_w, kb_l, vb_l, mqbT, mask, 0L, 0L,
-                pO2, pM2, pL2, N_REC, N_LIG, ns2);
-        } else {
-            attn_mfma<1><<<nb1 + nb2, 256, 0, stream>>>(
-                nb1,
-                h_lig, q_lig_w, kb_r, vb_r, (const unsigned long long*)0, mask, (long)N_REC, 1L,
-                pO1, pM1, pL1, N_LIG, N_REC, ns1,
-                h_rec, q_rec_w, kb_l, vb_l, (const unsigned long long*)0, mask, 1L, (long)N_REC,
-                pO2, pM2, pL2, N_REC, N_LIG, ns2);
-        }
+            pc_lig1, lig_cm_b1, lig_cm_w2, lig_cm_b2, aggr_l, xacc_l);
+
         attn_merge2<<<N_LIG + N_REC, 64, 0, stream>>>(
             pO1, pM1, pL1, h_lig_o, ns1, pO2, pM2, pL2, h_rec_o, ns2);
     } else {
-        attn_row_kernel<<<N_LIG, 256, N_REC * sizeof(float), stream>>>(
-            h_lig, q_lig_w, kb_r, vb_r, mask, (long)N_REC, 1L, h_lig_o, N_REC);
-        attn_row_kernel<<<N_REC, 256, N_LIG * sizeof(float), stream>>>(
-            h_rec, q_rec_w, kb_l, vb_l, mask, 1L, (long)N_REC, h_rec_o, N_LIG);
-    }
-
-    node_mfma<<<N_LIG / 64 + N_REC / 64, 256, 0, stream>>>(
-        N_LIG / 64,
+        edge_mfma_f<F_LIGc, 5><<<E_LIG / 64, 256, 0, stream>>>(
+            order_l, coords_lig, h_lig, lig_src, lig_dst, lig_efeat,
+            p_lig1, lig_em_b1, lig_em_g, lig_em_bt, p_lig2, lig_em_b2,
+            pc_lig1, lig_cm_b1, lig_cm_w2, lig_cm_b2, aggr_l, xacc_l);
+        edge_mfma_f<F_RECc, 6><<<E_REC / 64, 256, 0, stream>>>(
+            order_r, coords_rec, h_rec, rec_src, rec_dst, rec_efeat,
+            p_rec1, rec_em_b1, rec_em_g, rec_em_bt, p_rec2, rec_em_b2,
+            pc_rec1, rec_cm_b1, rec_cm_w2, rec_cm_b2, aggr_r, xacc_r);
+        if (tier == 1) {
+            attn_f32mask<<<nb1 + nb2, 256, 0, stream>>>(
+                nb1,
+                h_lig, q_lig_w, kb_r, vb_r, mask, (long)N_REC, 1L,
+                pO1, pM1, pL1, N_LIG, N_REC, ns1,
+                h_rec, q_rec_w, kb_l, vb_l, mask, 1L, (long)N_REC,
+                pO2, pM2, pL2, N_REC, N_LIG, ns2);
+            attn_merge2<<<N_LIG + N_REC, 64, 0, stream>>>(
+                pO1, pM1, pL1, h_lig_o, ns1, pO2, pM2, pL2, h_rec_o, ns2);
+        } else {
+            attn_row_kernel<<<N_LIG, 256, N_REC * sizeof(float), stream>>>(
+                h_lig, q_lig_w, kb_r, vb_r, mask, (long)N_REC, 1L, h_lig_o, N_REC);
+            attn_row_kernel<<<N_REC, 256, N_LIG * sizeof(float), stream>>>(
+                h_rec, q_rec_w, kb_l, vb_l, mask, 1L, (long)N_REC, h_rec_o, N_LIG);
+        }
+    }
+
+    const int nbn = N_LIG / 64 + N_REC / 64;
+    const int nbc = ((N_LIG + N_REC) * 3 + 255) / 256;
+    node_mfma<<<nbn + nbc, 256, 0, stream>>>(
+        N_LIG / 64, nbn,
         h_lig, aggr_l, counts_l, h_lig_o, orig_h_lig,
         lig_nm_w1, lig_nm_b1, lig_nm_g, lig_nm_bt, lig_nm_w2, lig_nm_b2, h_lig_o,
         h_rec, aggr_r, counts_r, h_rec_o, orig_h_rec,
-        rec_nm_w1, rec_nm_b1, rec_nm_g, rec_nm_bt, rec_nm_w2, rec_nm_b2, h_rec_o);
-
-    coord2_kernel<<<((N_LIG + N_REC) * 3 + 255) / 256, 256, 0, stream>>>(
-        orig_coords_lig, coords_lig, xacc_l, counts_l, x_lig_o,
-        orig_coords_rec, coords_rec, xacc_r, counts_r, x_rec_o);
-}
+        rec_nm_w1, rec_nm_b1, rec_nm_g, rec_nm_bt, rec_nm_w2, rec_nm_b2, h_rec_o,
+        orig_coords_lig, coords_lig, xacc_l, x_lig_o,
+        orig_coords_rec, coords_rec, xacc_r, x_rec_o);
+}
```

Result: no change. 605.7 us (-0.4%).
